# Kernel optimization log

Hardware: AMD Instinct MI355X
Metric: run time of the kernel (lower is better)

## Reference

```python
import jax, jax.numpy as jnp
import numpy as np

LN_EPS = 1e-9

def _layer_norm(x, g, b):
    mu = jnp.mean(x, axis=-1, keepdims=True)
    var = jnp.mean((x - mu) ** 2, axis=-1, keepdims=True)
    return (x - mu) * jax.lax.rsqrt(var + LN_EPS) * g + b

def _ffn(x, w1, b1, w2, b2, ln_g, ln_b):
    h = jax.nn.gelu(x @ w1 + b1, approximate=False)
    h = h @ w2 + b2
    return _layer_norm(h, ln_g, ln_b)

def _kernel_mean(x, y):
    d = x.shape[1]
    x2 = jnp.sum(x * x, axis=1)[:, None]
    y2 = jnp.sum(y * y, axis=1)[None, :]
    sq = x2 + y2 - 2.0 * (x @ y.T)  # [Nx, Ny]
    return jnp.mean(jnp.exp(-sq / (d * d)))

def _mmd(x, y):
    return _kernel_mean(x, x) + _kernel_mean(y, y) - 2.0 * _kernel_mean(x, y)

def setup_inputs() -> dict:
    key = jax.random.key(0)
    ks = jax.random.split(key, 8)
    B, S, D, DI, DL = 8, 512, 1024, 4096, 64
    s = lambda fan: 1.0 / np.sqrt(fan)
    return {
        "hidden": jax.random.normal(ks[0], (B, S, D), jnp.float32),
        "true_samples": jax.random.normal(ks[1], (B * S, DL), jnp.float32),
        "enc_w1": jax.random.normal(ks[2], (D, DI), jnp.float32) * s(D),
        "enc_b1": jnp.zeros((DI,), jnp.float32),
        "enc_w2": jax.random.normal(ks[3], (DI, DL), jnp.float32) * s(DI),
        "enc_b2": jnp.zeros((DL,), jnp.float32),
        "enc_ln_g": jnp.ones((DL,), jnp.float32),
        "enc_ln_b": jnp.zeros((DL,), jnp.float32),
        "dec_w1": jax.random.normal(ks[4], (DL, DI), jnp.float32) * s(DL),
        "dec_b1": jnp.zeros((DI,), jnp.float32),
        "dec_w2": jax.random.normal(ks[5], (DI, D), jnp.float32) * s(DI),
        "dec_b2": jnp.zeros((D,), jnp.float32),
        "dec_ln_g": jnp.ones((D,), jnp.float32),
        "dec_ln_b": jnp.zeros((D,), jnp.float32),
    }

def reference(hidden, true_samples, enc_w1, enc_b1, enc_w2, enc_b2, enc_ln_g, enc_ln_b,
              dec_w1, dec_b1, dec_w2, dec_b2, dec_ln_g, dec_ln_b):
    latent = _ffn(hidden, enc_w1, enc_b1, enc_w2, enc_b2, enc_ln_g, enc_ln_b)  # [B,S,DL]
    recon = _ffn(latent, dec_w1, dec_b1, dec_w2, dec_b2, dec_ln_g, dec_ln_b)   # [B,S,D]
    B, S, DL = latent.shape
    lat_flat = latent.reshape(-1, DL)  # [B*S, DL]
    reg_loss = _mmd(true_samples, lat_flat) / B * S
    return recon, latent, reg_loss
```

## Files before the change

### kernel.cpp

```cpp
#include <hip/hip_runtime.h>
#include <hip/hip_bf16.h>
#include <math.h>


typedef __attribute__((ext_vector_type(8))) short short8;
typedef __attribute__((ext_vector_type(4))) float float4a;
typedef __attribute__((ext_vector_type(4))) unsigned short us4;

__device__ inline ushort bf16r(float x) {
    union { float f; unsigned u; } c; c.f = x;
    unsigned r = (c.u + 0x7fffu + ((c.u >> 16) & 1u)) >> 16;
    return (ushort)r;
}

__device__ inline void gld_lds16(const void* g, void* l) {
    __builtin_amdgcn_global_load_lds(
        (const __attribute__((address_space(1))) void*)g,
        (__attribute__((address_space(3))) void*)l, 16, 0, 0);
}

template <int N> __device__ inline void wait_vmcnt() {
    if constexpr (N == 0) asm volatile("s_waitcnt vmcnt(0)" ::: "memory");
    else if constexpr (N == 4) asm volatile("s_waitcnt vmcnt(4)" ::: "memory");
    else if constexpr (N == 6) asm volatile("s_waitcnt vmcnt(6)" ::: "memory");
}

template <int N> __device__ inline void wait_lgkmcnt() {
    if constexpr (N == 0) asm volatile("s_waitcnt lgkmcnt(0)" ::: "memory");
    else if constexpr (N == 2) asm volatile("s_waitcnt lgkmcnt(2)" ::: "memory");
    else if constexpr (N == 4) asm volatile("s_waitcnt lgkmcnt(4)" ::: "memory");
    else if constexpr (N == 6) asm volatile("s_waitcnt lgkmcnt(6)" ::: "memory");
    else if constexpr (N == 8) asm volatile("s_waitcnt lgkmcnt(8)" ::: "memory");
    else if constexpr (N == 12) asm volatile("s_waitcnt lgkmcnt(12)" ::: "memory");
}

__device__ inline float fast_gelu(float v) {
    float v2 = v * v;
    float u = v * __builtin_fmaf(0.07135481627f, v2, 1.5957691216f);
    u = fminf(u, 30.0f);
    float e = __expf(u);
    return v * e * __builtin_amdgcn_rcpf(e + 1.0f);
}

__global__ __launch_bounds__(256) void k_pre(
        const float* __restrict__ hidden, ushort* __restrict__ A1bf,
        const float* __restrict__ tsamp, ushort* __restrict__ Tbf,
        float* __restrict__ sq_t, float* __restrict__ acc,
        const float* __restrict__ i0, ushort* __restrict__ o0,
        const float* __restrict__ i1, ushort* __restrict__ o1,
        const float* __restrict__ i2, ushort* __restrict__ o2,
        const float* __restrict__ i3, ushort* __restrict__ o3) {
    int b = blockIdx.x, tid = threadIdx.x;
    if (b == 0 && tid < 24) acc[tid] = 0.0f;
    if (b < 4096) {
        int i = b * 1024 + tid * 4;
        float4 v = *(const float4*)(hidden + i);
        us4 o = {bf16r(v.x), bf16r(v.y), bf16r(v.z), bf16r(v.w)};
        *(us4*)(A1bf + i) = o;
        return;
    }
    if (b < 4352) {
        int i = (b - 4096) * 1024 + tid * 4;
        float4 v = *(const float4*)(tsamp + i);
        us4 o = {bf16r(v.x), bf16r(v.y), bf16r(v.z), bf16r(v.w)};
        *(us4*)(Tbf + i) = o;
        float s = v.x * v.x + v.y * v.y + v.z * v.z + v.w * v.w;
#pragma unroll
        for (int off = 8; off; off >>= 1) s += __shfl_xor(s, off);
        if ((tid & 15) == 0) sq_t[i >> 6] = s;
        return;
    }
    __shared__ float t[32][65];
    const float* in; ushort* out; int R, C;
    int lb = b - 4352;
    if (lb < 2048)      { in = i0; out = o0; R = 1024; C = 4096; }
    else if (lb < 2176) { in = i1; out = o1; R = 4096; C = 64;   lb -= 2048; }
    else if (lb < 2304) { in = i2; out = o2; R = 64;   C = 4096; lb -= 2176; }
    else                { in = i3; out = o3; R = 4096; C = 1024; lb -= 2304; }
    int bx = (lb % (C / 32)) * 32;
    int by = (lb / (C / 32)) * 64;
    int tx = tid & 31, ty = tid >> 5;
#pragma unroll
    for (int i = 0; i < 64; i += 8)
        t[tx][i + ty] = in[(size_t)(by + i + ty) * C + (bx + tx)];
    __syncthreads();
#pragma unroll
    for (int i = 0; i < 32; i += 8) {
        int c = i + ty;
        ushort2 o;
        o.x = bf16r(t[c][2 * tx]);
        o.y = bf16r(t[c][2 * tx + 1]);
        *(ushort2*)(&out[(size_t)(bx + c) * R + by + 2 * tx]) = o;
    }
}

template <int BN, int EPI, bool SWZ>
__global__ __launch_bounds__(256) void k_gemm(
        const ushort* __restrict__ A, const ushort* __restrict__ Bt,
        const float* __restrict__ bias, void* __restrict__ Out,
        float* __restrict__ Out2, int M, int N, int K, int KC) {
    constexpr int BM = 128, BK = 64;
    constexpr int WAVES_N = BN / 64;
    constexpr int WAVES_M = 4 / WAVES_N;
    constexpr int WM = BM / WAVES_M;
    constexpr int MT = WM / 16;
    constexpr int NT = 4;
    constexpr int CA = BM / 32, CB = BN / 32;

    __shared__ ushort sA[BM * 64];
    __shared__ ushort sB[BN * 64];

    const int tid  = threadIdx.x;
    const int wave = tid >> 6, lane = tid & 63;
    const int wm = wave / WAVES_N, wn = wave % WAVES_N;
    int bx = blockIdx.x, by = blockIdx.y;
    if constexpr (SWZ) {
        int lin = blockIdx.x + gridDim.x * blockIdx.y;
        by = lin % gridDim.y;
        bx = lin / gridDim.y;
    }
    const int m0 = by * BM, n0 = bx * BN;
    const int lrow = lane & 15, lq = lane >> 4;
    const int srow8 = lane >> 3;
    const int sk8   = lane & 7;
    const int kbeg = blockIdx.z * KC;

    const ushort* pA[CA]; unsigned lA[CA];
#pragma unroll
    for (int j = 0; j < CA; ++j) {
        int c = wave * CA + j;
        int r = c * 8 + srow8;
        pA[j] = &A[(size_t)(m0 + r) * K + kbeg + ((sk8 ^ (r & 7)) * 8)];
        lA[j] = c * 512;
    }
    const ushort* pB[CB]; unsigned lB[CB];
#pragma unroll
    for (int j = 0; j < CB; ++j) {
        int c = wave * CB + j;
        int r = c * 8 + srow8;
        pB[j] = &Bt[(size_t)(n0 + r) * K + kbeg + ((sk8 ^ (r & 7)) * 8)];
        lB[j] = c * 512;
    }
    unsigned aoff[2][MT], boff[2][NT];
#pragma unroll
    for (int h = 0; h < 2; ++h) {
#pragma unroll
        for (int mt = 0; mt < MT; ++mt) {
            int r = wm * WM + mt * 16 + lrow;
            aoff[h][mt] = r * 64 + (((h * 4 + lq) ^ (r & 7)) * 8);
        }
#pragma unroll
        for (int nt = 0; nt < NT; ++nt) {
            int r = wn * 64 + nt * 16 + lrow;
            boff[h][nt] = r * 64 + (((h * 4 + lq) ^ (r & 7)) * 8);
        }
    }

    float4a acc[MT][NT];
#pragma unroll
    for (int mt = 0; mt < MT; ++mt)
#pragma unroll
        for (int nt = 0; nt < NT; ++nt)
            acc[mt][nt] = (float4a){0.f, 0.f, 0.f, 0.f};

    for (int k0 = 0; k0 < KC; k0 += BK) {
#pragma unroll
        for (int j = 0; j < CA; ++j) {
            gld_lds16(pA[j], &sA[lA[j]]);
            pA[j] += BK;
        }
#pragma unroll
        for (int j = 0; j < CB; ++j) {
            gld_lds16(pB[j], &sB[lB[j]]);
            pB[j] += BK;
        }
        __syncthreads();
#pragma unroll
        for (int h = 0; h < 2; ++h) {
            short8 af[MT], bfr[NT];
#pragma unroll
            for (int mt = 0; mt < MT; ++mt)
                af[mt] = *(short8*)(&sA[aoff[h][mt]]);
#pragma unroll
            for (int nt = 0; nt < NT; ++nt)
                bfr[nt] = *(short8*)(&sB[boff[h][nt]]);
#pragma unroll
            for (int mt = 0; mt < MT; ++mt)
#pragma unroll
                for (int nt = 0; nt < NT; ++nt)
                    acc[mt][nt] = __builtin_amdgcn_mfma_f32_16x16x32_bf16(
                        af[mt], bfr[nt], acc[mt][nt], 0, 0, 0);
        }
        __syncthreads();
    }

    float* dstp = nullptr;
    if constexpr (EPI == 2) {
        if (Out2 && blockIdx.z) dstp = Out2;
        else dstp = (float*)Out + (size_t)blockIdx.z * M * N;
    }
#pragma unroll
    for (int mt = 0; mt < MT; ++mt)
#pragma unroll
        for (int nt = 0; nt < NT; ++nt) {
            int col = n0 + wn * 64 + nt * 16 + lrow;
            float bv = 0.f;
            if constexpr (EPI != 2) bv = bias[col];
#pragma unroll
            for (int r = 0; r < 4; ++r) {
                int row = m0 + wm * WM + mt * 16 + lq * 4 + r;
                float v = acc[mt][nt][r] + bv;
                if constexpr (EPI == 0) {
                    ((ushort*)Out)[(size_t)row * N + col] = bf16r(fast_gelu(v));
                } else if constexpr (EPI == 1) {
                    ((float*)Out)[(size_t)row * N + col] = v;
                } else {
                    dstp[(size_t)row * N + col] = v;
                }
            }
        }
}

template <int BN, int EPI, int CX, int CY>
__global__ __launch_bounds__(512, 2) void k_gemm256mb(
        const ushort* __restrict__ A, const ushort* __restrict__ Bt,
        const float* __restrict__ bias, void* __restrict__ Out,
        float* __restrict__ Out2, int M, int N, int K, int KC) {
    constexpr int BM = 256, BK = 64;
    constexpr int AI = 4;
    constexpr int BI = BN / 64;
    constexpr int WAVES_N = BN / 64;
    constexpr int WAVES_M = 8 / WAVES_N;
    constexpr int WM = BM / WAVES_M;
    constexpr int MT = WM / 16;
    constexpr int NT = 4;

    __shared__ ushort sA[2][BM * 64];
    __shared__ ushort sB[2][BN * 64];

    const int tid = threadIdx.x;
    const int wave = tid >> 6, lane = tid & 63;
    const int wm = wave / WAVES_N, wn = wave % WAVES_N;

    const int gx = gridDim.x, gy = gridDim.y;
    const int lin = blockIdx.x + gx * (blockIdx.y + gy * blockIdx.z);
    const int nwg = gx * gy * gridDim.z;
    const int cpx = nwg >> 3;
    const int swz = (lin & 7) * cpx + (lin >> 3);
    const int nz  = gx * gy;
    const int zz  = swz / nz;
    const int rr  = swz % nz;
    const int chunk = rr / (CX * CY);
    const int lcl   = rr % (CX * CY);
    const int ncx   = gx / CX;
    const int bx = (chunk % ncx) * CX + (lcl % CX);
    const int by = (chunk / ncx) * CY + (lcl / CX);

    const int m0 = by * BM, n0 = bx * BN;
    const int lrow = lane & 15, lq = lane >> 4;
    const int kbeg = zz * KC;
    const int nT = KC / BK;

    const int crow = tid >> 3;
    const int ck8  = (tid & 7) ^ (crow & 7);
    const ushort* pAbase = A  + (size_t)(m0 + crow) * K + kbeg + ck8 * 8;
    const ushort* pBbase = Bt + (size_t)(n0 + crow) * K + kbeg + ck8 * 8;

    const int a0  = (wm * WM + lrow) * 64;
    const int b0  = (wn * 64 + lrow) * 64;
    const int sw0 = ((lq) ^ (lrow & 7)) * 8;
    const int sw1 = ((4 + lq) ^ (lrow & 7)) * 8;

    float4a acc[MT][NT];
#pragma unroll
    for (int mt = 0; mt < MT; ++mt)
#pragma unroll
        for (int nt = 0; nt < NT; ++nt)
            acc[mt][nt] = (float4a){0.f, 0.f, 0.f, 0.f};

#pragma unroll
    for (int j = 0; j < AI; ++j)
        gld_lds16(pAbase + (size_t)j * 64 * K, &sA[0][j * 4096 + wave * 512]);
#pragma unroll
    for (int j = 0; j < BI; ++j)
        gld_lds16(pBbase + (size_t)j * 64 * K, &sB[0][j * 4096 + wave * 512]);
    wait_vmcnt<0>();
    __builtin_amdgcn_s_barrier();
    __builtin_amdgcn_sched_barrier(0);

    for (int t = 0; t < nT; ++t) {
        const int d = t & 1;
        const bool pf1 = (t + 1 < nT);
        const size_t koff1 = (size_t)(t + 1) * BK;

        short8 af0[MT], bfr0[NT], af1[MT], bfr1[NT];
#pragma unroll
        for (int mt = 0; mt < MT; ++mt)
            af0[mt] = *(const short8*)(&sA[d][a0 + mt * 1024 + sw0]);
#pragma unroll
        for (int nt = 0; nt < NT; ++nt)
            bfr0[nt] = *(const short8*)(&sB[d][b0 + nt * 1024 + sw0]);
        __builtin_amdgcn_sched_barrier(0);
#pragma unroll
        for (int mt = 0; mt < MT; ++mt)
            af1[mt] = *(const short8*)(&sA[d][a0 + mt * 1024 + sw1]);
#pragma unroll
        for (int nt = 0; nt < NT; ++nt)
            bfr1[nt] = *(const short8*)(&sB[d][b0 + nt * 1024 + sw1]);
        if (pf1) {
#pragma unroll
            for (int j = 0; j < AI; ++j)
                gld_lds16(pAbase + (size_t)j * 64 * K + koff1,
                          &sA[d ^ 1][j * 4096 + wave * 512]);
#pragma unroll
            for (int j = 0; j < BI; ++j)
                gld_lds16(pBbase + (size_t)j * 64 * K + koff1,
                          &sB[d ^ 1][j * 4096 + wave * 512]);
        }
        wait_lgkmcnt<MT + 4>();
        __builtin_amdgcn_sched_barrier(0);
        __builtin_amdgcn_s_setprio(1);
#pragma unroll
        for (int mt = 0; mt < MT; ++mt)
#pragma unroll
            for (int nt = 0; nt < NT; ++nt)
                acc[mt][nt] = __builtin_amdgcn_mfma_f32_16x16x32_bf16(
                    af0[mt], bfr0[nt], acc[mt][nt], 0, 0, 0);
        __builtin_amdgcn_s_setprio(0);
        wait_lgkmcnt<0>();
        __builtin_amdgcn_sched_barrier(0);
        __builtin_amdgcn_s_setprio(1);
#pragma unroll
        for (int mt = 0; mt < MT; ++mt)
#pragma unroll
            for (int nt = 0; nt < NT; ++nt)
                acc[mt][nt] = __builtin_amdgcn_mfma_f32_16x16x32_bf16(
                    af1[mt], bfr1[nt], acc[mt][nt], 0, 0, 0);
        __builtin_amdgcn_s_setprio(0);
        if (pf1) {
            wait_vmcnt<0>();
            __builtin_amdgcn_s_barrier();
            __builtin_amdgcn_sched_barrier(0);
        }
    }

    float* dstp = nullptr;
    if constexpr (EPI == 2) {
        if (Out2 && zz) dstp = Out2;
        else dstp = (float*)Out + (size_t)zz * M * N;
    }
#pragma unroll
    for (int mt = 0; mt < MT; ++mt)
#pragma unroll
        for (int nt = 0; nt < NT; ++nt) {
            const int col = n0 + wn * 64 + nt * 16 + lrow;
            float bv = 0.f;
            if constexpr (EPI == 0) bv = bias[col];
#pragma unroll
            for (int r = 0; r < 4; ++r) {
                const int row = m0 + wm * WM + mt * 16 + lq * 4 + r;
                float v = acc[mt][nt][r] + bv;
                if constexpr (EPI == 0)
                    ((ushort*)Out)[(size_t)row * N + col] = bf16r(fast_gelu(v));
                else
                    dstp[(size_t)row * N + col] = v;
            }
        }
}

__global__ __launch_bounds__(512, 2) void k_gemm1f(
        const ushort* __restrict__ A, const ushort* __restrict__ Bt,
        const float* __restrict__ bias, const ushort* __restrict__ W2t,
        float* __restrict__ part, int M, int N, int K) {
    constexpr int BM = 256, BN = 256, BK = 64;
    constexpr int AI = 4, BI = 4;
    constexpr int WAVES_N = 4;
    constexpr int WM = 128;
    constexpr int MT = 8, NT = 4;
    constexpr int CX = 4, CY = 8;

    __shared__ ushort smem[65536];

    const int tid = threadIdx.x;
    const int wave = tid >> 6, lane = tid & 63;
    const int wm = wave / WAVES_N, wn = wave % WAVES_N;

    const int gx = gridDim.x, gy = gridDim.y;
    const int lin = blockIdx.x + gx * blockIdx.y;
    const int cpx = (gx * gy) >> 3;
    const int swz = (lin & 7) * cpx + (lin >> 3);
    const int chunk = swz / (CX * CY);
    const int lcl   = swz % (CX * CY);
    const int ncx   = gx / CX;
    const int bx = (chunk % ncx) * CX + (lcl % CX);
    const int by = (chunk / ncx) * CY + (lcl / CX);

    const int m0 = by * BM, n0 = bx * BN;
    const int lrow = lane & 15, lq = lane >> 4;
    const int nT = K / BK;

    const int crow = tid >> 3;
    const int ck8  = (tid & 7) ^ (crow & 7);
    const ushort* pAbase = A  + (size_t)(m0 + crow) * K + ck8 * 8;
    const ushort* pBbase = Bt + (size_t)(n0 + crow) * K + ck8 * 8;

    const int a0  = (wm * WM + lrow) * 64;
    const int b0  = (wn * 64 + lrow) * 64;
    const int sw0 = ((lq) ^ (lrow & 7)) * 8;
    const int sw1 = ((4 + lq) ^ (lrow & 7)) * 8;

    float4a acc[MT][NT];
#pragma unroll
    for (int mt = 0; mt < MT; ++mt)
#pragma unroll
        for (int nt = 0; nt < NT; ++nt)
            acc[mt][nt] = (float4a){0.f, 0.f, 0.f, 0.f};

#pragma unroll
    for (int j = 0; j < AI; ++j)
        gld_lds16(pAbase + (size_t)j * 64 * K, &smem[j * 4096 + wave * 512]);
#pragma unroll
    for (int j = 0; j < BI; ++j)
        gld_lds16(pBbase + (size_t)j * 64 * K,
                  &smem[32768 + j * 4096 + wave * 512]);
    wait_vmcnt<0>();
    __builtin_amdgcn_s_barrier();
    __builtin_amdgcn_sched_barrier(0);

    for (int t = 0; t < nT; ++t) {
        const int d = t & 1;
        const bool pf1 = (t + 1 < nT);
        const size_t koff1 = (size_t)(t + 1) * BK;
        const ushort* sAd = &smem[d * 16384];
        const ushort* sBd = &smem[32768 + d * 16384];

        short8 af0[MT], bfr0[NT], af1[MT], bfr1[NT];
#pragma unroll
        for (int mt = 0; mt < MT; ++mt)
            af0[mt] = *(const short8*)(&sAd[a0 + mt * 1024 + sw0]);
#pragma unroll
        for (int nt = 0; nt < NT; ++nt)
            bfr0[nt] = *(const short8*)(&sBd[b0 + nt * 1024 + sw0]);
        __builtin_amdgcn_sched_barrier(0);
#pragma unroll
        for (int mt = 0; mt < MT; ++mt)
            af1[mt] = *(const short8*)(&sAd[a0 + mt * 1024 + sw1]);
#pragma unroll
        for (int nt = 0; nt < NT; ++nt)
            bfr1[nt] = *(const short8*)(&sBd[b0 + nt * 1024 + sw1]);
        if (pf1) {
#pragma unroll
            for (int j = 0; j < AI; ++j)
                gld_lds16(pAbase + (size_t)j * 64 * K + koff1,
                          &smem[(d ^ 1) * 16384 + j * 4096 + wave * 512]);
#pragma unroll
            for (int j = 0; j < BI; ++j)
                gld_lds16(pBbase + (size_t)j * 64 * K + koff1,
                          &smem[32768 + (d ^ 1) * 16384 + j * 4096 + wave * 512]);
        }
        wait_lgkmcnt<12>();
        __builtin_amdgcn_sched_barrier(0);
        __builtin_amdgcn_s_setprio(1);
#pragma unroll
        for (int mt = 0; mt < MT; ++mt)
#pragma unroll
            for (int nt = 0; nt < NT; ++nt)
                acc[mt][nt] = __builtin_amdgcn_mfma_f32_16x16x32_bf16(
                    af0[mt], bfr0[nt], acc[mt][nt], 0, 0, 0);
        __builtin_amdgcn_s_setprio(0);
        wait_lgkmcnt<0>();
        __builtin_amdgcn_sched_barrier(0);
        __builtin_amdgcn_s_setprio(1);
#pragma unroll
        for (int mt = 0; mt < MT; ++mt)
#pragma unroll
            for (int nt = 0; nt < NT; ++nt)
                acc[mt][nt] = __builtin_amdgcn_mfma_f32_16x16x32_bf16(
                    af1[mt], bfr1[nt], acc[mt][nt], 0, 0, 0);
        __builtin_amdgcn_s_setprio(0);
        if (pf1) {
            wait_vmcnt<0>();
            __builtin_amdgcn_s_barrier();
            __builtin_amdgcn_sched_barrier(0);
        }
    }

    __syncthreads();
#pragma unroll
    for (int mt = 0; mt < MT; ++mt)
#pragma unroll
        for (int nt = 0; nt < NT; ++nt) {
            const int c = wn * 64 + nt * 16 + lrow;
            const float bv = bias[n0 + c];
            const int s = c >> 3, cl = c & 7;
#pragma unroll
            for (int r_ = 0; r_ < 4; ++r_) {
                const int r = wm * WM + mt * 16 + lq * 4 + r_;
                const int sz = (s & 24) | ((s & 7) ^ (r & 7));
                smem[r * 256 + sz * 8 + cl] =
                    bf16r(fast_gelu(acc[mt][nt][r_] + bv));
            }
        }
    __syncthreads();

    float4a pacc[2][4];
#pragma unroll
    for (int m2 = 0; m2 < 2; ++m2)
#pragma unroll
        for (int n2 = 0; n2 < 4; ++n2)
            pacc[m2][n2] = (float4a){0.f, 0.f, 0.f, 0.f};

    const ushort* gW2 = W2t + n0;
#pragma unroll
    for (int kk = 0; kk < 8; ++kk) {
        short8 af2[2], bf2[4];
#pragma unroll
        for (int m2 = 0; m2 < 2; ++m2) {
            const int r2 = wave * 32 + m2 * 16 + lrow;
            const int s2 = kk * 4 + lq;
            const int sz2 = (s2 & 24) | ((s2 & 7) ^ (r2 & 7));
            af2[m2] = *(const short8*)(&smem[r2 * 256 + sz2 * 8]);
        }
#pragma unroll
        for (int n2 = 0; n2 < 4; ++n2) {
            const int l = n2 * 16 + lrow;
            bf2[n2] = *(const short8*)(&gW2[(size_t)l * 4096 + kk * 32 + lq * 8]);
        }
#pragma unroll
        for (int m2 = 0; m2 < 2; ++m2)
#pragma unroll
            for (int n2 = 0; n2 < 4; ++n2)
                pacc[m2][n2] = __builtin_amdgcn_mfma_f32_16x16x32_bf16(
                    af2[m2], bf2[n2], pacc[m2][n2], 0, 0, 0);
    }

    float* pz = part + (size_t)bx * M * 64;
#pragma unroll
    for (int m2 = 0; m2 < 2; ++m2)
#pragma unroll
        for (int n2 = 0; n2 < 4; ++n2) {
            const int lat = n2 * 16 + lrow;
#pragma unroll
            for (int r_ = 0; r_ < 4; ++r_) {
                const int row = m0 + wave * 32 + m2 * 16 + lq * 4 + r_;
                pz[(size_t)row * 64 + lat] = pacc[m2][n2][r_];
            }
        }
}

__global__ __launch_bounds__(256) void k_gram_all(
        const ushort* __restrict__ Tbf, const ushort* __restrict__ Lbf,
        const float* __restrict__ sq_t, const float* __restrict__ sq_l,
        float* __restrict__ accum) {
    __shared__ ushort sX[128 * 64];
    __shared__ ushort sY[128 * 64];
    __shared__ float red[4];

    int id = blockIdx.x;
    int pair, tbx, tby; float w;
    if (id < 1056) {
        pair = (id < 528) ? 0 : 1;
        int t = (pair == 0) ? id : id - 528;
        int r = (int)((sqrtf(8.0f * t + 1.0f) - 1.0f) * 0.5f);
        while ((r + 1) * (r + 2) / 2 <= t) ++r;
        while (r * (r + 1) / 2 > t) --r;
        tby = r; tbx = t - r * (r + 1) / 2;
        w = (tbx == tby) ? 1.0f : 2.0f;
    } else {
        pair = 2; int t = id - 1056;
        tbx = t & 31; tby = t >> 5; w = 1.0f;
    }
    const ushort* Xb = (pair == 1) ? Lbf : Tbf;
    const ushort* Yb = (pair == 0) ? Tbf : Lbf;
    const float* sqX = (pair == 1) ? sq_l : sq_t;
    const float* sqY = (pair == 0) ? sq_t : sq_l;

    const int tid  = threadIdx.x;
    const int wave = tid >> 6, lane = tid & 63;
    const int wm = wave >> 1, wn = wave & 1;
    const int bx = tbx * 128, by = tby * 128;
    const int lrow = lane & 15, lq = lane >> 4;
    const int srow8 = lane >> 3, sk8 = lane & 7;

#pragma unroll
    for (int j = 0; j < 4; ++j) {
        int c = wave * 4 + j;
        int r = c * 8 + srow8;
        int kc = (sk8 ^ (r & 7)) * 8;
        gld_lds16(&Xb[(size_t)(bx + r) * 64 + kc], &sX[c * 512]);
        gld_lds16(&Yb[(size_t)(by + r) * 64 + kc], &sY[c * 512]);
    }

    unsigned xoff[2][4], yoff[2][4];
#pragma unroll
    for (int h = 0; h < 2; ++h)
#pragma unroll
        for (int i = 0; i < 4; ++i) {
            int rx = wm * 64 + i * 16 + lrow;
            int ry = wn * 64 + i * 16 + lrow;
            xoff[h][i] = rx * 64 + (((h * 4 + lq) ^ (rx & 7)) * 8);
            yoff[h][i] = ry * 64 + (((h * 4 + lq) ^ (ry & 7)) * 8);
        }
    __syncthreads();

    float4a acc[4][4];
#pragma unroll
    for (int mt = 0; mt < 4; ++mt)
#pragma unroll
        for (int nt = 0; nt < 4; ++nt)
            acc[mt][nt] = (float4a){0.f, 0.f, 0.f, 0.f};

#pragma unroll
    for (int h = 0; h < 2; ++h) {
        short8 xf[4], yf[4];
#pragma unroll
        for (int mt = 0; mt < 4; ++mt)
            xf[mt] = *(short8*)(&sX[xoff[h][mt]]);
#pragma unroll
        for (int nt = 0; nt < 4; ++nt)
            yf[nt] = *(short8*)(&sY[yoff[h][nt]]);
#pragma unroll
        for (int mt = 0; mt < 4; ++mt)
#pragma unroll
            for (int nt = 0; nt < 4; ++nt)
                acc[mt][nt] = __builtin_amdgcn_mfma_f32_16x16x32_bf16(
                    xf[mt], yf[nt], acc[mt][nt], 0, 0, 0);
    }

    float sy[4];
#pragma unroll
    for (int nt = 0; nt < 4; ++nt)
        sy[nt] = sqY[by + wn * 64 + nt * 16 + lrow];
    float s = 0.f;
#pragma unroll
    for (int mt = 0; mt < 4; ++mt)
#pragma unroll
        for (int r = 0; r < 4; ++r) {
            float sx = sqX[bx + wm * 64 + mt * 16 + lq * 4 + r];
#pragma unroll
            for (int nt = 0; nt < 4; ++nt)
                s += __expf((2.0f * acc[mt][nt][r] - sx - sy[nt]) * (1.0f / 4096.0f));
        }
    s *= w;
#pragma unroll
    for (int off = 32; off; off >>= 1) s += __shfl_xor(s, off);
    if ((tid & 63) == 0) red[tid >> 6] = s;
    __syncthreads();
    if (tid == 0) atomicAdd(accum + pair * 8, red[0] + red[1] + red[2] + red[3]);
}

__global__ __launch_bounds__(256) void k_ln64_red(
        const float* __restrict__ part, int npart,
        const float* __restrict__ bias, const float* __restrict__ g,
        const float* __restrict__ b, float* __restrict__ outf,
        ushort* __restrict__ outb, float* __restrict__ sq_l) {
    int wave = threadIdx.x >> 6, lane = threadIdx.x & 63;
    int row = blockIdx.x * 4 + wave;
    float x = bias[lane];
    for (int s = 0; s < npart; ++s)
        x += part[(size_t)s * 4096 * 64 + row * 64 + lane];
    float s = x;
#pragma unroll
    for (int off = 32; off; off >>= 1) s += __shfl_xor(s, off);
    float mu = s * (1.0f / 64.0f);
    float d = x - mu;
    float v = d * d;
#pragma unroll
    for (int off = 32; off; off >>= 1) v += __shfl_xor(v, off);
    float rs = rsqrtf(v * (1.0f / 64.0f) + 1e-9f);
    float y = d * rs * g[lane] + b[lane];
    outf[row * 64 + lane] = y;
    outb[row * 64 + lane] = bf16r(y);
    float q = y * y;
#pragma unroll
    for (int off = 32; off; off >>= 1) q += __shfl_xor(q, off);
    if (lane == 0) sq_l[row] = q;
}

__global__ __launch_bounds__(256) void k_ln1024_red(
        const float* __restrict__ p0, const float* __restrict__ p1,
        const float* __restrict__ bias, const float* __restrict__ g,
        const float* __restrict__ b, float* __restrict__ out) {
    __shared__ float red[4];
    int row = blockIdx.x, tid = threadIdx.x;
    const float4 v0 = *(const float4*)(p0 + (size_t)row * 1024 + tid * 4);
    const float4 v1 = *(const float4*)(p1 + (size_t)row * 1024 + tid * 4);
    const float4 bb = *(const float4*)(bias + tid * 4);
    float4 v;
    v.x = v0.x + v1.x + bb.x;
    v.y = v0.y + v1.y + bb.y;
    v.z = v0.z + v1.z + bb.z;
    v.w = v0.w + v1.w + bb.w;
    float s = v.x + v.y + v.z + v.w;
#pragma unroll
    for (int off = 32; off; off >>= 1) s += __shfl_xor(s, off);
    if ((tid & 63) == 0) red[tid >> 6] = s;
    __syncthreads();
    float mu = (red[0] + red[1] + red[2] + red[3]) * (1.0f / 1024.0f);
    float dx = v.x - mu, dy = v.y - mu, dz = v.z - mu, dw = v.w - mu;
    float q = dx * dx + dy * dy + dz * dz + dw * dw;
#pragma unroll
    for (int off = 32; off; off >>= 1) q += __shfl_xor(q, off);
    __syncthreads();
    if ((tid & 63) == 0) red[tid >> 6] = q;
    __syncthreads();
    float rs = rsqrtf((red[0] + red[1] + red[2] + red[3]) * (1.0f / 1024.0f) + 1e-9f);
    const float4 gv = *(const float4*)(g + tid * 4);
    const float4 bv = *(const float4*)(b + tid * 4);
    float4 o;
    o.x = dx * rs * gv.x + bv.x;
    o.y = dy * rs * gv.y + bv.y;
    o.z = dz * rs * gv.z + bv.z;
    o.w = dw * rs * gv.w + bv.w;
    *(float4*)(out + (size_t)row * 1024 + tid * 4) = o;
}

__global__ void k_finalize(const float* __restrict__ accum, float* __restrict__ out) {
    out[0] = (accum[0] + accum[8] - 2.0f * accum[16]) * (64.0f / (4096.0f * 4096.0f));
}

extern "C" void kernel_launch(void* const* d_in, const int* in_sizes, int n_in,
                              void* d_out, int out_size, void* d_ws, size_t ws_size,
                              hipStream_t stream) {
    const float* hidden   = (const float*)d_in[0];
    const float* tsamp    = (const float*)d_in[1];
    const float* enc_w1   = (const float*)d_in[2];
    const float* enc_b1   = (const float*)d_in[3];
    const float* enc_w2   = (const float*)d_in[4];
    const float* enc_b2   = (const float*)d_in[5];
    const float* enc_ln_g = (const float*)d_in[6];
    const float* enc_ln_b = (const float*)d_in[7];
    const float* dec_w1   = (const float*)d_in[8];
    const float* dec_b1   = (const float*)d_in[9];
    const float* dec_w2   = (const float*)d_in[10];
    const float* dec_b2   = (const float*)d_in[11];
    const float* dec_ln_g = (const float*)d_in[12];
    const float* dec_ln_b = (const float*)d_in[13];

    float* out      = (float*)d_out;
    float* recon    = out;
    float* latent_f = out + 4194304;
    float* reg      = out + 4456448;

    char* ws = (char*)d_ws;
    const size_t MB = 1024 * 1024;
    ushort* A1bf = (ushort*)(ws + 0);
    ushort* W1t  = (ushort*)(ws + 8 * MB);
    float*  h4p0 = (float*)(ws + 0);
    ushort* H1bf = (ushort*)(ws + 16 * MB);
    float*  part = (float*)(ws + 16 * MB);
    ushort* W4t  = (ushort*)(ws + 48 * MB);
    ushort* W2t  = (ushort*)(ws + 56 * MB);
    ushort* W3t  = (ushort*)(ws + 56 * MB + 512 * 1024);
    ushort* Lbf  = (ushort*)(ws + 57 * MB);
    float*  sq_t = (float*)(ws + 59 * MB);
    float*  sq_l = (float*)(ws + 59 * MB + 16384);
    float*  acc3 = (float*)(ws + 59 * MB + 32768);
    ushort* Tbf  = (ushort*)(ws + 59 * MB + 65536);

    k_pre<<<8704, 256, 0, stream>>>(hidden, A1bf, tsamp, Tbf, sq_t, acc3,
                                    enc_w1, W1t, enc_w2, W2t,
                                    dec_w1, W3t, dec_w2, W4t);

    k_gemm1f<<<dim3(16, 16, 1), 512, 0, stream>>>(
        A1bf, W1t, enc_b1, W2t, part, 4096, 4096, 1024);
    k_ln64_red<<<1024, 256, 0, stream>>>(part, 16, enc_b2, enc_ln_g, enc_ln_b,
                                         latent_f, Lbf, sq_l);

    k_gemm<64, 0, false><<<dim3(64, 32, 1), 256, 0, stream>>>(
        Lbf, W3t, dec_b1, H1bf, nullptr, 4096, 4096, 64, 64);
    k_gemm256mb<128, 2, 8, 4><<<dim3(8, 16, 2), 512, 0, stream>>>(
        H1bf, W4t, nullptr, h4p0, recon, 4096, 1024, 4096, 2048);
    k_ln1024_red<<<4096, 256, 0, stream>>>(h4p0, recon, dec_b2, dec_ln_g,
                                           dec_ln_b, recon);

    k_gram_all<<<2080, 256, 0, stream>>>(Tbf, Lbf, sq_t, sq_l, acc3);
    k_finalize<<<1, 1, 0, stream>>>(acc3, reg);
}
```

Before: 260.6 us.

## Fuse whole pipeline into one cooperative persistent kernel with grid syncs

```diff
diff --git a/kernel.cpp b/kernel.cpp
--- a/kernel.cpp
+++ b/kernel.cpp
@@ -1,7 +1,10 @@
 #include <hip/hip_runtime.h>
+#include <hip/hip_cooperative_groups.h>
 #include <hip/hip_bf16.h>
 #include <math.h>
 
+
+namespace cg = cooperative_groups;
 
 typedef __attribute__((ext_vector_type(8))) short short8;
 typedef __attribute__((ext_vector_type(4))) float float4a;
@@ -21,16 +24,10 @@
 
 template <int N> __device__ inline void wait_vmcnt() {
     if constexpr (N == 0) asm volatile("s_waitcnt vmcnt(0)" ::: "memory");
-    else if constexpr (N == 4) asm volatile("s_waitcnt vmcnt(4)" ::: "memory");
-    else if constexpr (N == 6) asm volatile("s_waitcnt vmcnt(6)" ::: "memory");
 }
 
 template <int N> __device__ inline void wait_lgkmcnt() {
     if constexpr (N == 0) asm volatile("s_waitcnt lgkmcnt(0)" ::: "memory");
-    else if constexpr (N == 2) asm volatile("s_waitcnt lgkmcnt(2)" ::: "memory");
-    else if constexpr (N == 4) asm volatile("s_waitcnt lgkmcnt(4)" ::: "memory");
-    else if constexpr (N == 6) asm volatile("s_waitcnt lgkmcnt(6)" ::: "memory");
-    else if constexpr (N == 8) asm volatile("s_waitcnt lgkmcnt(8)" ::: "memory");
     else if constexpr (N == 12) asm volatile("s_waitcnt lgkmcnt(12)" ::: "memory");
 }
 
@@ -42,681 +39,631 @@
     return v * e * __builtin_amdgcn_rcpf(e + 1.0f);
 }
 
-__global__ __launch_bounds__(256) void k_pre(
-        const float* __restrict__ hidden, ushort* __restrict__ A1bf,
-        const float* __restrict__ tsamp, ushort* __restrict__ Tbf,
-        float* __restrict__ sq_t, float* __restrict__ acc,
-        const float* __restrict__ i0, ushort* __restrict__ o0,
-        const float* __restrict__ i1, ushort* __restrict__ o1,
-        const float* __restrict__ i2, ushort* __restrict__ o2,
-        const float* __restrict__ i3, ushort* __restrict__ o3) {
-    int b = blockIdx.x, tid = threadIdx.x;
-    if (b == 0 && tid < 24) acc[tid] = 0.0f;
-    if (b < 4096) {
-        int i = b * 1024 + tid * 4;
-        float4 v = *(const float4*)(hidden + i);
-        us4 o = {bf16r(v.x), bf16r(v.y), bf16r(v.z), bf16r(v.w)};
-        *(us4*)(A1bf + i) = o;
-        return;
+__global__ __launch_bounds__(512, 2) void k_mega(
+        const float* __restrict__ hidden, const float* __restrict__ tsamp,
+        const float* __restrict__ ew1, const float* __restrict__ eb1,
+        const float* __restrict__ ew2, const float* __restrict__ eb2,
+        const float* __restrict__ elng, const float* __restrict__ elnb,
+        const float* __restrict__ dw1, const float* __restrict__ db1,
+        const float* __restrict__ dw2, const float* __restrict__ db2,
+        const float* __restrict__ dlng, const float* __restrict__ dlnb,
+        float* __restrict__ recon, float* __restrict__ latent_f,
+        float* __restrict__ regout,
+        ushort* __restrict__ A1bf, ushort* __restrict__ W1t,
+        float* __restrict__ part, float* __restrict__ h4p0,
+        ushort* __restrict__ H1bf, ushort* __restrict__ W4t,
+        ushort* __restrict__ W2t, ushort* __restrict__ W3t,
+        ushort* __restrict__ Lbf, float* __restrict__ sq_t,
+        float* __restrict__ sq_l, float* __restrict__ acc3,
+        ushort* __restrict__ Tbf) {
+    __shared__ char smem_u[131072];
+    cg::grid_group grid = cg::this_grid();
+
+    const int bid = blockIdx.x;
+    const int tid = threadIdx.x;
+    const int wave = tid >> 6, lane = tid & 63;
+    const int htid = tid & 255, half = tid >> 8;
+    const int lrow = lane & 15, lq = lane >> 4;
+    const int srow8 = lane >> 3, sk8 = lane & 7;
+
+    {
+        if (bid == 0 && tid < 32) acc3[tid] = 0.0f;
+#pragma unroll
+        for (int it = 0; it < 8; ++it) {
+            int i4 = it * 131072 + bid * 512 + tid;
+            float4 v = ((const float4*)hidden)[i4];
+            us4 o = {bf16r(v.x), bf16r(v.y), bf16r(v.z), bf16r(v.w)};
+            ((us4*)A1bf)[i4] = o;
+        }
+        {
+            int gw = bid * 8 + wave;
+            if (gw < 1024) {
+                int row = gw * 4 + (lane >> 4);
+                int i = row * 64 + (lane & 15) * 4;
+                float4 v = *(const float4*)(tsamp + i);
+                us4 o = {bf16r(v.x), bf16r(v.y), bf16r(v.z), bf16r(v.w)};
+                *(us4*)(Tbf + i) = o;
+                float s = v.x * v.x + v.y * v.y + v.z * v.z + v.w * v.w;
+#pragma unroll
+                for (int off = 8; off; off >>= 1) s += __shfl_xor(s, off);
+                if ((lane & 15) == 0) sq_t[row] = s;
+            }
+        }
+        float (*tT)[65] = (float(*)[65])(smem_u + half * 8320);
+        int tx = htid & 31, ty = htid >> 5;
+        for (int it = 0; it < 9; ++it) {
+            int vt = (bid + it * 256) * 2 + half;
+            bool act = vt < 4352;
+            const float* in = nullptr; ushort* out = nullptr; int R = 1, C = 32;
+            int lb = vt;
+            if (act) {
+                if (lb < 2048)      { in = ew1; out = W1t; R = 1024; C = 4096; }
+                else if (lb < 2176) { in = ew2; out = W2t; R = 4096; C = 64;   lb -= 2048; }
+                else if (lb < 2304) { in = dw1; out = W3t; R = 64;   C = 4096; lb -= 2176; }
+                else                { in = dw2; out = W4t; R = 4096; C = 1024; lb -= 2304; }
+            }
+            int bx = act ? (lb % (C / 32)) * 32 : 0;
+            int by = act ? (lb / (C / 32)) * 64 : 0;
+            if (act) {
+#pragma unroll
+                for (int i = 0; i < 64; i += 8)
+                    tT[tx][i + ty] = in[(size_t)(by + i + ty) * C + (bx + tx)];
+            }
+            __syncthreads();
+            if (act) {
+#pragma unroll
+                for (int i = 0; i < 32; i += 8) {
+                    int c = i + ty;
+                    ushort2 o;
+                    o.x = bf16r(tT[c][2 * tx]);
+                    o.y = bf16r(tT[c][2 * tx + 1]);
+                    *(ushort2*)(&out[(size_t)(bx + c) * R + by + 2 * tx]) = o;
+                }
+            }
+            __syncthreads();
+        }
     }
-    if (b < 4352) {
-        int i = (b - 4096) * 1024 + tid * 4;
-        float4 v = *(const float4*)(tsamp + i);
-        us4 o = {bf16r(v.x), bf16r(v.y), bf16r(v.z), bf16r(v.w)};
-        *(us4*)(Tbf + i) = o;
-        float s = v.x * v.x + v.y * v.y + v.z * v.z + v.w * v.w;
-#pragma unroll
-        for (int off = 8; off; off >>= 1) s += __shfl_xor(s, off);
-        if ((tid & 15) == 0) sq_t[i >> 6] = s;
-        return;
-    }
-    __shared__ float t[32][65];
-    const float* in; ushort* out; int R, C;
-    int lb = b - 4352;
-    if (lb < 2048)      { in = i0; out = o0; R = 1024; C = 4096; }
-    else if (lb < 2176) { in = i1; out = o1; R = 4096; C = 64;   lb -= 2048; }
-    else if (lb < 2304) { in = i2; out = o2; R = 64;   C = 4096; lb -= 2176; }
-    else                { in = i3; out = o3; R = 4096; C = 1024; lb -= 2304; }
-    int bx = (lb % (C / 32)) * 32;
-    int by = (lb / (C / 32)) * 64;
-    int tx = tid & 31, ty = tid >> 5;
-#pragma unroll
-    for (int i = 0; i < 64; i += 8)
-        t[tx][i + ty] = in[(size_t)(by + i + ty) * C + (bx + tx)];
-    __syncthreads();
-#pragma unroll
-    for (int i = 0; i < 32; i += 8) {
-        int c = i + ty;
-        ushort2 o;
-        o.x = bf16r(t[c][2 * tx]);
-        o.y = bf16r(t[c][2 * tx + 1]);
-        *(ushort2*)(&out[(size_t)(bx + c) * R + by + 2 * tx]) = o;
-    }
-}
-
-template <int BN, int EPI, bool SWZ>
-__global__ __launch_bounds__(256) void k_gemm(
-        const ushort* __restrict__ A, const ushort* __restrict__ Bt,
-        const float* __restrict__ bias, void* __restrict__ Out,
-        float* __restrict__ Out2, int M, int N, int K, int KC) {
-    constexpr int BM = 128, BK = 64;
-    constexpr int WAVES_N = BN / 64;
-    constexpr int WAVES_M = 4 / WAVES_N;
-    constexpr int WM = BM / WAVES_M;
-    constexpr int MT = WM / 16;
-    constexpr int NT = 4;
-    constexpr int CA = BM / 32, CB = BN / 32;
-
-    __shared__ ushort sA[BM * 64];
-    __shared__ ushort sB[BN * 64];
-
-    const int tid  = threadIdx.x;
-    const int wave = tid >> 6, lane = tid & 63;
-    const int wm = wave / WAVES_N, wn = wave % WAVES_N;
-    int bx = blockIdx.x, by = blockIdx.y;
-    if constexpr (SWZ) {
-        int lin = blockIdx.x + gridDim.x * blockIdx.y;
-        by = lin % gridDim.y;
-        bx = lin / gridDim.y;
-    }
-    const int m0 = by * BM, n0 = bx * BN;
-    const int lrow = lane & 15, lq = lane >> 4;
-    const int srow8 = lane >> 3;
-    const int sk8   = lane & 7;
-    const int kbeg = blockIdx.z * KC;
-
-    const ushort* pA[CA]; unsigned lA[CA];
-#pragma unroll
-    for (int j = 0; j < CA; ++j) {
-        int c = wave * CA + j;
-        int r = c * 8 + srow8;
-        pA[j] = &A[(size_t)(m0 + r) * K + kbeg + ((sk8 ^ (r & 7)) * 8)];
-        lA[j] = c * 512;
-    }
-    const ushort* pB[CB]; unsigned lB[CB];
-#pragma unroll
-    for (int j = 0; j < CB; ++j) {
-        int c = wave * CB + j;
-        int r = c * 8 + srow8;
-        pB[j] = &Bt[(size_t)(n0 + r) * K + kbeg + ((sk8 ^ (r & 7)) * 8)];
-        lB[j] = c * 512;
-    }
-    unsigned aoff[2][MT], boff[2][NT];
-#pragma unroll
-    for (int h = 0; h < 2; ++h) {
-#pragma unroll
-        for (int mt = 0; mt < MT; ++mt) {
-            int r = wm * WM + mt * 16 + lrow;
-            aoff[h][mt] = r * 64 + (((h * 4 + lq) ^ (r & 7)) * 8);
-        }
-#pragma unroll
-        for (int nt = 0; nt < NT; ++nt) {
-            int r = wn * 64 + nt * 16 + lrow;
-            boff[h][nt] = r * 64 + (((h * 4 + lq) ^ (r & 7)) * 8);
-        }
-    }
-
-    float4a acc[MT][NT];
-#pragma unroll
-    for (int mt = 0; mt < MT; ++mt)
-#pragma unroll
-        for (int nt = 0; nt < NT; ++nt)
-            acc[mt][nt] = (float4a){0.f, 0.f, 0.f, 0.f};
-
-    for (int k0 = 0; k0 < KC; k0 += BK) {
-#pragma unroll
-        for (int j = 0; j < CA; ++j) {
-            gld_lds16(pA[j], &sA[lA[j]]);
-            pA[j] += BK;
-        }
-#pragma unroll
-        for (int j = 0; j < CB; ++j) {
-            gld_lds16(pB[j], &sB[lB[j]]);
-            pB[j] += BK;
-        }
-        __syncthreads();
-#pragma unroll
-        for (int h = 0; h < 2; ++h) {
-            short8 af[MT], bfr[NT];
+    __threadfence();
+    grid.sync();
+
+    {
+        constexpr int AI = 4, BI = 4, MT = 8, NT = 4;
+        constexpr int WM = 128, CX = 4, CY = 8;
+        ushort* smem = (ushort*)smem_u;
+        const int wm = wave / 4, wn = wave % 4;
+        const int lin = bid;
+        const int cpx = 256 >> 3;
+        const int swz = (lin & 7) * cpx + (lin >> 3);
+        const int chunk = swz / (CX * CY);
+        const int lcl   = swz % (CX * CY);
+        const int ncx   = 16 / CX;
+        const int bx = (chunk % ncx) * CX + (lcl % CX);
+        const int by = (chunk / ncx) * CY + (lcl / CX);
+        const int m0 = by * 256, n0 = bx * 256;
+        const int K = 1024, nT = 16;
+
+        const int crow = tid >> 3;
+        const int ck8  = (tid & 7) ^ (crow & 7);
+        const ushort* pAbase = A1bf + (size_t)(m0 + crow) * K + ck8 * 8;
+        const ushort* pBbase = W1t  + (size_t)(n0 + crow) * K + ck8 * 8;
+
+        const int a0  = (wm * WM + lrow) * 64;
+        const int b0  = (wn * 64 + lrow) * 64;
+        const int sw0 = ((lq) ^ (lrow & 7)) * 8;
+        const int sw1 = ((4 + lq) ^ (lrow & 7)) * 8;
+
+        float4a acc[MT][NT];
+#pragma unroll
+        for (int mt = 0; mt < MT; ++mt)
+#pragma unroll
+            for (int nt = 0; nt < NT; ++nt)
+                acc[mt][nt] = (float4a){0.f, 0.f, 0.f, 0.f};
+
+#pragma unroll
+        for (int j = 0; j < AI; ++j)
+            gld_lds16(pAbase + (size_t)j * 64 * K, &smem[j * 4096 + wave * 512]);
+#pragma unroll
+        for (int j = 0; j < BI; ++j)
+            gld_lds16(pBbase + (size_t)j * 64 * K,
+                      &smem[32768 + j * 4096 + wave * 512]);
+        wait_vmcnt<0>();
+        __builtin_amdgcn_s_barrier();
+        __builtin_amdgcn_sched_barrier(0);
+
+        for (int t = 0; t < nT; ++t) {
+            const int d = t & 1;
+            const bool pf1 = (t + 1 < nT);
+            const size_t koff1 = (size_t)(t + 1) * 64;
+            const ushort* sAd = &smem[d * 16384];
+            const ushort* sBd = &smem[32768 + d * 16384];
+
+            short8 af0[MT], bfr0[NT], af1[MT], bfr1[NT];
 #pragma unroll
             for (int mt = 0; mt < MT; ++mt)
-                af[mt] = *(short8*)(&sA[aoff[h][mt]]);
+                af0[mt] = *(const short8*)(&sAd[a0 + mt * 1024 + sw0]);
 #pragma unroll
             for (int nt = 0; nt < NT; ++nt)
-                bfr[nt] = *(short8*)(&sB[boff[h][nt]]);
+                bfr0[nt] = *(const short8*)(&sBd[b0 + nt * 1024 + sw0]);
+            __builtin_amdgcn_sched_barrier(0);
+#pragma unroll
+            for (int mt = 0; mt < MT; ++mt)
+                af1[mt] = *(const short8*)(&sAd[a0 + mt * 1024 + sw1]);
+#pragma unroll
+            for (int nt = 0; nt < NT; ++nt)
+                bfr1[nt] = *(const short8*)(&sBd[b0 + nt * 1024 + sw1]);
+            if (pf1) {
+#pragma unroll
+                for (int j = 0; j < AI; ++j)
+                    gld_lds16(pAbase + (size_t)j * 64 * K + koff1,
+                              &smem[(d ^ 1) * 16384 + j * 4096 + wave * 512]);
+#pragma unroll
+                for (int j = 0; j < BI; ++j)
+                    gld_lds16(pBbase + (size_t)j * 64 * K + koff1,
+                              &smem[32768 + (d ^ 1) * 16384 + j * 4096 + wave * 512]);
+            }
+            wait_lgkmcnt<12>();
+            __builtin_amdgcn_sched_barrier(0);
+            __builtin_amdgcn_s_setprio(1);
 #pragma unroll
             for (int mt = 0; mt < MT; ++mt)
 #pragma unroll
                 for (int nt = 0; nt < NT; ++nt)
                     acc[mt][nt] = __builtin_amdgcn_mfma_f32_16x16x32_bf16(
-                        af[mt], bfr[nt], acc[mt][nt], 0, 0, 0);
-        }
+                        af0[mt], bfr0[nt], acc[mt][nt], 0, 0, 0);
+            __builtin_amdgcn_s_setprio(0);
+            wait_lgkmcnt<0>();
+            __builtin_amdgcn_sched_barrier(0);
+            __builtin_amdgcn_s_setprio(1);
+#pragma unroll
+            for (int mt = 0; mt < MT; ++mt)
+#pragma unroll
+                for (int nt = 0; nt < NT; ++nt)
+                    acc[mt][nt] = __builtin_amdgcn_mfma_f32_16x16x32_bf16(
+                        af1[mt], bfr1[nt], acc[mt][nt], 0, 0, 0);
+            __builtin_amdgcn_s_setprio(0);
+            if (pf1) {
+                wait_vmcnt<0>();
+                __builtin_amdgcn_s_barrier();
+                __builtin_amdgcn_sched_barrier(0);
+            }
+        }
+
         __syncthreads();
+#pragma unroll
+        for (int mt = 0; mt < MT; ++mt)
+#pragma unroll
+            for (int nt = 0; nt < NT; ++nt) {
+                const int c = wn * 64 + nt * 16 + lrow;
+                const float bv = eb1[n0 + c];
+                const int s = c >> 3, cl = c & 7;
+#pragma unroll
+                for (int r_ = 0; r_ < 4; ++r_) {
+                    const int r = wm * WM + mt * 16 + lq * 4 + r_;
+                    const int sz = (s & 24) | ((s & 7) ^ (r & 7));
+                    smem[r * 256 + sz * 8 + cl] =
+                        bf16r(fast_gelu(acc[mt][nt][r_] + bv));
+                }
+            }
+        __syncthreads();
+
+        float4a pacc[2][4];
+#pragma unroll
+        for (int m2 = 0; m2 < 2; ++m2)
+#pragma unroll
+            for (int n2 = 0; n2 < 4; ++n2)
+                pacc[m2][n2] = (float4a){0.f, 0.f, 0.f, 0.f};
+
+        const ushort* gW2 = W2t + n0;
+#pragma unroll
+        for (int kk = 0; kk < 8; ++kk) {
+            short8 af2[2], bf2[4];
+#pragma unroll
+            for (int m2 = 0; m2 < 2; ++m2) {
+                const int r2 = wave * 32 + m2 * 16 + lrow;
+                const int s2 = kk * 4 + lq;
+                const int sz2 = (s2 & 24) | ((s2 & 7) ^ (r2 & 7));
+                af2[m2] = *(const short8*)(&smem[r2 * 256 + sz2 * 8]);
+            }
+#pragma unroll
+            for (int n2 = 0; n2 < 4; ++n2) {
+                const int l = n2 * 16 + lrow;
+                bf2[n2] = *(const short8*)(&gW2[(size_t)l * 4096 + kk * 32 + lq * 8]);
+            }
+#pragma unroll
+            for (int m2 = 0; m2 < 2; ++m2)
+#pragma unroll
+                for (int n2 = 0; n2 < 4; ++n2)
+                    pacc[m2][n2] = __builtin_amdgcn_mfma_f32_16x16x32_bf16(
+                        af2[m2], bf2[n2], pacc[m2][n2], 0, 0, 0);
+        }
+
+        float* pz = part + (size_t)bx * 4096 * 64;
+#pragma unroll
+        for (int m2 = 0; m2 < 2; ++m2)
+#pragma unroll
+            for (int n2 = 0; n2 < 4; ++n2) {
+                const int lat = n2 * 16 + lrow;
+#pragma unroll
+                for (int r_ = 0; r_ < 4; ++r_) {
+                    const int row = m0 + wave * 32 + m2 * 16 + lq * 4 + r_;
+                    pz[(size_t)row * 64 + lat] = pacc[m2][n2][r_];
+                }
+            }
     }
-
-    float* dstp = nullptr;
-    if constexpr (EPI == 2) {
-        if (Out2 && blockIdx.z) dstp = Out2;
-        else dstp = (float*)Out + (size_t)blockIdx.z * M * N;
+    __threadfence();
+    grid.sync();
+
+    {
+        int gw = bid * 8 + wave;
+#pragma unroll
+        for (int rr = 0; rr < 2; ++rr) {
+            int row = gw + rr * 2048;
+            float x = eb2[lane];
+            for (int s = 0; s < 16; ++s)
+                x += part[(size_t)s * 4096 * 64 + row * 64 + lane];
+            float s = x;
+#pragma unroll
+            for (int off = 32; off; off >>= 1) s += __shfl_xor(s, off);
+            float mu = s * (1.0f / 64.0f);
+            float dxx = x - mu;
+            float v = dxx * dxx;
+#pragma unroll
+            for (int off = 32; off; off >>= 1) v += __shfl_xor(v, off);
+            float rs = rsqrtf(v * (1.0f / 64.0f) + 1e-9f);
+            float y = dxx * rs * elng[lane] + elnb[lane];
+            latent_f[row * 64 + lane] = y;
+            Lbf[row * 64 + lane] = bf16r(y);
+            float q = y * y;
+#pragma unroll
+            for (int off = 32; off; off >>= 1) q += __shfl_xor(q, off);
+            if (lane == 0) sq_l[row] = q;
+        }
     }
-#pragma unroll
-    for (int mt = 0; mt < MT; ++mt)
-#pragma unroll
-        for (int nt = 0; nt < NT; ++nt) {
-            int col = n0 + wn * 64 + nt * 16 + lrow;
-            float bv = 0.f;
-            if constexpr (EPI != 2) bv = bias[col];
-#pragma unroll
-            for (int r = 0; r < 4; ++r) {
-                int row = m0 + wm * WM + mt * 16 + lq * 4 + r;
-                float v = acc[mt][nt][r] + bv;
-                if constexpr (EPI == 0) {
-                    ((ushort*)Out)[(size_t)row * N + col] = bf16r(fast_gelu(v));
-                } else if constexpr (EPI == 1) {
-                    ((float*)Out)[(size_t)row * N + col] = v;
+    __threadfence();
+    grid.sync();
+
+    {
+        ushort* sA3 = (ushort*)(smem_u + half * 24576);
+        ushort* sB3 = sA3 + 8192;
+        const int w4 = htid >> 6, hl = htid & 63;
+        const int hlrow = hl & 15, hlq = hl >> 4;
+        const int hsr8 = hl >> 3, hsk8 = hl & 7;
+        for (int it = 0; it < 4; ++it) {
+            int vt = (bid * 2 + half) + it * 512;
+            int bx3 = vt & 63, by3 = vt >> 6;
+            int m0 = by3 * 128, n0 = bx3 * 64;
+#pragma unroll
+            for (int j = 0; j < 4; ++j) {
+                int c = w4 * 4 + j;
+                int r = c * 8 + hsr8;
+                gld_lds16(&Lbf[(size_t)(m0 + r) * 64 + ((hsk8 ^ (r & 7)) * 8)],
+                          &sA3[c * 512]);
+            }
+#pragma unroll
+            for (int j = 0; j < 2; ++j) {
+                int c = w4 * 2 + j;
+                int r = c * 8 + hsr8;
+                gld_lds16(&W3t[(size_t)(n0 + r) * 64 + ((hsk8 ^ (r & 7)) * 8)],
+                          &sB3[c * 512]);
+            }
+            __syncthreads();
+            float4a a3[2][4];
+#pragma unroll
+            for (int mt = 0; mt < 2; ++mt)
+#pragma unroll
+                for (int nt = 0; nt < 4; ++nt)
+                    a3[mt][nt] = (float4a){0.f, 0.f, 0.f, 0.f};
+#pragma unroll
+            for (int h = 0; h < 2; ++h) {
+                short8 af[2], bfr[4];
+#pragma unroll
+                for (int mt = 0; mt < 2; ++mt) {
+                    int r = w4 * 32 + mt * 16 + hlrow;
+                    af[mt] = *(short8*)(&sA3[r * 64 + (((h * 4 + hlq) ^ (r & 7)) * 8)]);
+                }
+#pragma unroll
+                for (int nt = 0; nt < 4; ++nt) {
+                    int r = nt * 16 + hlrow;
+                    bfr[nt] = *(short8*)(&sB3[r * 64 + (((h * 4 + hlq) ^ (r & 7)) * 8)]);
+                }
+#pragma unroll
+                for (int mt = 0; mt < 2; ++mt)
+#pragma unroll
+                    for (int nt = 0; nt < 4; ++nt)
+                        a3[mt][nt] = __builtin_amdgcn_mfma_f32_16x16x32_bf16(
+                            af[mt], bfr[nt], a3[mt][nt], 0, 0, 0);
+            }
+            __syncthreads();
+#pragma unroll
+            for (int mt = 0; mt < 2; ++mt)
+#pragma unroll
+                for (int nt = 0; nt < 4; ++nt) {
+                    int col = n0 + nt * 16 + hlrow;
+                    float bv = db1[col];
+#pragma unroll
+                    for (int r_ = 0; r_ < 4; ++r_) {
+                        int row = m0 + w4 * 32 + mt * 16 + hlq * 4 + r_;
+                        H1bf[(size_t)row * 4096 + col] =
+                            bf16r(fast_gelu(a3[mt][nt][r_] + bv));
+                    }
+                }
+        }
+    }
+    __threadfence();
+    grid.sync();
+
+    {
+        constexpr int AI = 4, BI = 2, MT = 4, NT = 4, WM = 64;
+        constexpr int CX = 8, CY = 4;
+        ushort* sA4 = (ushort*)smem_u;
+        ushort* sB4 = (ushort*)(smem_u + 65536);
+        const int wm = wave / 2, wn = wave % 2;
+        const int gx = 8, gy = 16;
+        const int lin = bid;
+        const int cpx = 256 >> 3;
+        const int swz = (lin & 7) * cpx + (lin >> 3);
+        const int nz  = gx * gy;
+        const int zz  = swz / nz;
+        const int rr  = swz % nz;
+        const int chunk = rr / (CX * CY);
+        const int lcl   = rr % (CX * CY);
+        const int ncx   = gx / CX;
+        const int bx = (chunk % ncx) * CX + (lcl % CX);
+        const int by = (chunk / ncx) * CY + (lcl / CX);
+        const int m0 = by * 256, n0 = bx * 128;
+        const int K = 4096, KC = 2048, nT = 32;
+        const int kbeg = zz * KC;
+
+        const int crow = tid >> 3;
+        const int ck8  = (tid & 7) ^ (crow & 7);
+        const ushort* pAbase = H1bf + (size_t)(m0 + crow) * K + kbeg + ck8 * 8;
+        const ushort* pBbase = W4t  + (size_t)(n0 + crow) * K + kbeg + ck8 * 8;
+
+        const int a0  = (wm * WM + lrow) * 64;
+        const int b0  = (wn * 64 + lrow) * 64;
+        const int sw0 = ((lq) ^ (lrow & 7)) * 8;
+        const int sw1 = ((4 + lq) ^ (lrow & 7)) * 8;
+
+        float4a acc[MT][NT];
+#pragma unroll
+        for (int mt = 0; mt < MT; ++mt)
+#pragma unroll
+            for (int nt = 0; nt < NT; ++nt)
+                acc[mt][nt] = (float4a){0.f, 0.f, 0.f, 0.f};
+
+#pragma unroll
+        for (int j = 0; j < AI; ++j)
+            gld_lds16(pAbase + (size_t)j * 64 * K, &sA4[j * 4096 + wave * 512]);
+#pragma unroll
+        for (int j = 0; j < BI; ++j)
+            gld_lds16(pBbase + (size_t)j * 64 * K, &sB4[j * 4096 + wave * 512]);
+        wait_vmcnt<0>();
+        __builtin_amdgcn_s_barrier();
+        __builtin_amdgcn_sched_barrier(0);
+
+        for (int t = 0; t < nT; ++t) {
+            const int d = t & 1;
+            const bool pf1 = (t + 1 < nT);
+            const size_t koff1 = (size_t)(t + 1) * 64;
+            const ushort* sAd = &sA4[d * 16384];
+            const ushort* sBd = &sB4[d * 8192];
+
+            short8 af0[MT], bfr0[NT], af1[MT], bfr1[NT];
+#pragma unroll
+            for (int mt = 0; mt < MT; ++mt)
+                af0[mt] = *(const short8*)(&sAd[a0 + mt * 1024 + sw0]);
+#pragma unroll
+            for (int nt = 0; nt < NT; ++nt)
+                bfr0[nt] = *(const short8*)(&sBd[b0 + nt * 1024 + sw0]);
+            __builtin_amdgcn_sched_barrier(0);
+#pragma unroll
+            for (int mt = 0; mt < MT; ++mt)
+                af1[mt] = *(const short8*)(&sAd[a0 + mt * 1024 + sw1]);
+#pragma unroll
+            for (int nt = 0; nt < NT; ++nt)
+                bfr1[nt] = *(const short8*)(&sBd[b0 + nt * 1024 + sw1]);
+            if (pf1) {
+#pragma unroll
+                for (int j = 0; j < AI; ++j)
+                    gld_lds16(pAbase + (size_t)j * 64 * K + koff1,
+                              &sA4[(d ^ 1) * 16384 + j * 4096 + wave * 512]);
+#pragma unroll
+                for (int j = 0; j < BI; ++j)
+                    gld_lds16(pBbase + (size_t)j * 64 * K + koff1,
+                              &sB4[(d ^ 1) * 8192 + j * 4096 + wave * 512]);
+            }
+            wait_lgkmcnt<12>();
+            __builtin_amdgcn_sched_barrier(0);
+            __builtin_amdgcn_s_setprio(1);
+#pragma unroll
+            for (int mt = 0; mt < MT; ++mt)
+#pragma unroll
+                for (int nt = 0; nt < NT; ++nt)
+                    acc[mt][nt] = __builtin_amdgcn_mfma_f32_16x16x32_bf16(
+                        af0[mt], bfr0[nt], acc[mt][nt], 0, 0, 0);
+            __builtin_amdgcn_s_setprio(0);
+            wait_lgkmcnt<0>();
+            __builtin_amdgcn_sched_barrier(0);
+            __builtin_amdgcn_s_setprio(1);
+#pragma unroll
+            for (int mt = 0; mt < MT; ++mt)
+#pragma unroll
+                for (int nt = 0; nt < NT; ++nt)
+                    acc[mt][nt] = __builtin_amdgcn_mfma_f32_16x16x32_bf16(
+                        af1[mt], bfr1[nt], acc[mt][nt], 0, 0, 0);
+            __builtin_amdgcn_s_setprio(0);
+            if (pf1) {
+                wait_vmcnt<0>();
+                __builtin_amdgcn_s_barrier();
+                __builtin_amdgcn_sched_barrier(0);
+            }
+        }
+
+        float* dstp = zz ? recon : h4p0;
+#pragma unroll
+        for (int mt = 0; mt < MT; ++mt)
+#pragma unroll
+            for (int nt = 0; nt < NT; ++nt) {
+                const int col = n0 + wn * 64 + nt * 16 + lrow;
+#pragma unroll
+                for (int r_ = 0; r_ < 4; ++r_) {
+                    const int row = m0 + wm * WM + mt * 16 + lq * 4 + r_;
+                    dstp[(size_t)row * 1024 + col] = acc[mt][nt][r_];
+                }
+            }
+    }
+    __threadfence();
+    grid.sync();
+
+    {
+        float* red5 = (float*)smem_u + half * 4;
+        for (int it = 0; it < 8; ++it) {
+            int row = (bid * 2 + half) + it * 512;
+            const float4 v0 = *(const float4*)(h4p0 + (size_t)row * 1024 + htid * 4);
+            const float4 v1 = *(const float4*)(recon + (size_t)row * 1024 + htid * 4);
+            const float4 bb = *(const float4*)(db2 + htid * 4);
+            float4 v;
+            v.x = v0.x + v1.x + bb.x;
+            v.y = v0.y + v1.y + bb.y;
+            v.z = v0.z + v1.z + bb.z;
+            v.w = v0.w + v1.w + bb.w;
+            float s = v.x + v.y + v.z + v.w;
+#pragma unroll
+            for (int off = 32; off; off >>= 1) s += __shfl_xor(s, off);
+            if ((htid & 63) == 0) red5[htid >> 6] = s;
+            __syncthreads();
+            float mu = (red5[0] + red5[1] + red5[2] + red5[3]) * (1.0f / 1024.0f);
+            float dx = v.x - mu, dy = v.y - mu, dz = v.z - mu, dw = v.w - mu;
+            float q = dx * dx + dy * dy + dz * dz + dw * dw;
+#pragma unroll
+            for (int off = 32; off; off >>= 1) q += __shfl_xor(q, off);
+            __syncthreads();
+            if ((htid & 63) == 0) red5[htid >> 6] = q;
+            __syncthreads();
+            float rs = rsqrtf((red5[0] + red5[1] + red5[2] + red5[3]) *
+                              (1.0f / 1024.0f) + 1e-9f);
+            const float4 gv = *(const float4*)(dlng + htid * 4);
+            const float4 bv = *(const float4*)(dlnb + htid * 4);
+            float4 o;
+            o.x = dx * rs * gv.x + bv.x;
+            o.y = dy * rs * gv.y + bv.y;
+            o.z = dz * rs * gv.z + bv.z;
+            o.w = dw * rs * gv.w + bv.w;
+            *(float4*)(recon + (size_t)row * 1024 + htid * 4) = o;
+            __syncthreads();
+        }
+    }
+    __threadfence();
+    grid.sync();
+
+    {
+        ushort* sX = (ushort*)(smem_u + half * 32768);
+        ushort* sY = sX + 8192;
+        float* red6 = (float*)(smem_u + 65536) + half * 4;
+        const int w4 = htid >> 6, hl = htid & 63;
+        const int hlrow = hl & 15, hlq = hl >> 4;
+        const int hsr8 = hl >> 3, hsk8 = hl & 7;
+        const int wmg = w4 >> 1, wng = w4 & 1;
+
+        for (int it = 0; it < 5; ++it) {
+            int id = (bid * 2 + half) + it * 512;
+            bool act = id < 2080;
+            int pair = 0, tbx = 0, tby = 0; float w = 1.0f;
+            const ushort *Xb = Tbf, *Yb = Tbf;
+            const float *sqX = sq_t, *sqY = sq_t;
+            if (act) {
+                if (id < 1056) {
+                    pair = (id < 528) ? 0 : 1;
+                    int t = (pair == 0) ? id : id - 528;
+                    int r = (int)((sqrtf(8.0f * t + 1.0f) - 1.0f) * 0.5f);
+                    while ((r + 1) * (r + 2) / 2 <= t) ++r;
+                    while (r * (r + 1) / 2 > t) --r;
+                    tby = r; tbx = t - r * (r + 1) / 2;
+                    w = (tbx == tby) ? 1.0f : 2.0f;
                 } else {
-                    dstp[(size_t)row * N + col] = v;
-                }
-            }
-        }
-}
-
-template <int BN, int EPI, int CX, int CY>
-__global__ __launch_bounds__(512, 2) void k_gemm256mb(
-        const ushort* __restrict__ A, const ushort* __restrict__ Bt,
-        const float* __restrict__ bias, void* __restrict__ Out,
-        float* __restrict__ Out2, int M, int N, int K, int KC) {
-    constexpr int BM = 256, BK = 64;
-    constexpr int AI = 4;
-    constexpr int BI = BN / 64;
-    constexpr int WAVES_N = BN / 64;
-    constexpr int WAVES_M = 8 / WAVES_N;
-    constexpr int WM = BM / WAVES_M;
-    constexpr int MT = WM / 16;
-    constexpr int NT = 4;
-
-    __shared__ ushort sA[2][BM * 64];
-    __shared__ ushort sB[2][BN * 64];
-
-    const int tid = threadIdx.x;
-    const int wave = tid >> 6, lane = tid & 63;
-    const int wm = wave / WAVES_N, wn = wave % WAVES_N;
-
-    const int gx = gridDim.x, gy = gridDim.y;
-    const int lin = blockIdx.x + gx * (blockIdx.y + gy * blockIdx.z);
-    const int nwg = gx * gy * gridDim.z;
-    const int cpx = nwg >> 3;
-    const int swz = (lin & 7) * cpx + (lin >> 3);
-    const int nz  = gx * gy;
-    const int zz  = swz / nz;
-    const int rr  = swz % nz;
-    const int chunk = rr / (CX * CY);
-    const int lcl   = rr % (CX * CY);
-    const int ncx   = gx / CX;
-    const int bx = (chunk % ncx) * CX + (lcl % CX);
-    const int by = (chunk / ncx) * CY + (lcl / CX);
-
-    const int m0 = by * BM, n0 = bx * BN;
-    const int lrow = lane & 15, lq = lane >> 4;
-    const int kbeg = zz * KC;
-    const int nT = KC / BK;
-
-    const int crow = tid >> 3;
-    const int ck8  = (tid & 7) ^ (crow & 7);
-    const ushort* pAbase = A  + (size_t)(m0 + crow) * K + kbeg + ck8 * 8;
-    const ushort* pBbase = Bt + (size_t)(n0 + crow) * K + kbeg + ck8 * 8;
-
-    const int a0  = (wm * WM + lrow) * 64;
-    const int b0  = (wn * 64 + lrow) * 64;
-    const int sw0 = ((lq) ^ (lrow & 7)) * 8;
-    const int sw1 = ((4 + lq) ^ (lrow & 7)) * 8;
-
-    float4a acc[MT][NT];
-#pragma unroll
-    for (int mt = 0; mt < MT; ++mt)
-#pragma unroll
-        for (int nt = 0; nt < NT; ++nt)
-            acc[mt][nt] = (float4a){0.f, 0.f, 0.f, 0.f};
-
-#pragma unroll
-    for (int j = 0; j < AI; ++j)
-        gld_lds16(pAbase + (size_t)j * 64 * K, &sA[0][j * 4096 + wave * 512]);
-#pragma unroll
-    for (int j = 0; j < BI; ++j)
-        gld_lds16(pBbase + (size_t)j * 64 * K, &sB[0][j * 4096 + wave * 512]);
-    wait_vmcnt<0>();
-    __builtin_amdgcn_s_barrier();
-    __builtin_amdgcn_sched_barrier(0);
-
-    for (int t = 0; t < nT; ++t) {
-        const int d = t & 1;
-        const bool pf1 = (t + 1 < nT);
-        const size_t koff1 = (size_t)(t + 1) * BK;
-
-        short8 af0[MT], bfr0[NT], af1[MT], bfr1[NT];
-#pragma unroll
-        for (int mt = 0; mt < MT; ++mt)
-            af0[mt] = *(const short8*)(&sA[d][a0 + mt * 1024 + sw0]);
-#pragma unroll
-        for (int nt = 0; nt < NT; ++nt)
-            bfr0[nt] = *(const short8*)(&sB[d][b0 + nt * 1024 + sw0]);
-        __builtin_amdgcn_sched_barrier(0);
-#pragma unroll
-        for (int mt = 0; mt < MT; ++mt)
-            af1[mt] = *(const short8*)(&sA[d][a0 + mt * 1024 + sw1]);
-#pragma unroll
-        for (int nt = 0; nt < NT; ++nt)
-            bfr1[nt] = *(const short8*)(&sB[d][b0 + nt * 1024 + sw1]);
-        if (pf1) {
-#pragma unroll
-            for (int j = 0; j < AI; ++j)
-                gld_lds16(pAbase + (size_t)j * 64 * K + koff1,
-                          &sA[d ^ 1][j * 4096 + wave * 512]);
-#pragma unroll
-            for (int j = 0; j < BI; ++j)
-                gld_lds16(pBbase + (size_t)j * 64 * K + koff1,
-                          &sB[d ^ 1][j * 4096 + wave * 512]);
-        }
-        wait_lgkmcnt<MT + 4>();
-        __builtin_amdgcn_sched_barrier(0);
-        __builtin_amdgcn_s_setprio(1);
-#pragma unroll
-        for (int mt = 0; mt < MT; ++mt)
-#pragma unroll
-            for (int nt = 0; nt < NT; ++nt)
-                acc[mt][nt] = __builtin_amdgcn_mfma_f32_16x16x32_bf16(
-                    af0[mt], bfr0[nt], acc[mt][nt], 0, 0, 0);
-        __builtin_amdgcn_s_setprio(0);
-        wait_lgkmcnt<0>();
-        __builtin_amdgcn_sched_barrier(0);
-        __builtin_amdgcn_s_setprio(1);
-#pragma unroll
-        for (int mt = 0; mt < MT; ++mt)
-#pragma unroll
-            for (int nt = 0; nt < NT; ++nt)
-                acc[mt][nt] = __builtin_amdgcn_mfma_f32_16x16x32_bf16(
-                    af1[mt], bfr1[nt], acc[mt][nt], 0, 0, 0);
-        __builtin_amdgcn_s_setprio(0);
-        if (pf1) {
-            wait_vmcnt<0>();
-            __builtin_amdgcn_s_barrier();
-            __builtin_amdgcn_sched_barrier(0);
+                    pair = 2; int t = id - 1056;
+                    tbx = t & 31; tby = t >> 5; w = 1.0f;
+                }
+                Xb = (pair == 1) ? Lbf : Tbf;
+                Yb = (pair == 0) ? Tbf : Lbf;
+                sqX = (pair == 1) ? sq_l : sq_t;
+                sqY = (pair == 0) ? sq_t : sq_l;
+            }
+            const int bx = tbx * 128, by = tby * 128;
+            if (act) {
+#pragma unroll
+                for (int j = 0; j < 4; ++j) {
+                    int c = w4 * 4 + j;
+                    int r = c * 8 + hsr8;
+                    int kc = (hsk8 ^ (r & 7)) * 8;
+                    gld_lds16(&Xb[(size_t)(bx + r) * 64 + kc], &sX[c * 512]);
+                    gld_lds16(&Yb[(size_t)(by + r) * 64 + kc], &sY[c * 512]);
+                }
+            }
+            __syncthreads();
+            float s = 0.f;
+            if (act) {
+                float4a ag[4][4];
+#pragma unroll
+                for (int mt = 0; mt < 4; ++mt)
+#pragma unroll
+                    for (int nt = 0; nt < 4; ++nt)
+                        ag[mt][nt] = (float4a){0.f, 0.f, 0.f, 0.f};
+#pragma unroll
+                for (int h = 0; h < 2; ++h) {
+                    short8 xf[4], yf[4];
+#pragma unroll
+                    for (int mt = 0; mt < 4; ++mt) {
+                        int rx = wmg * 64 + mt * 16 + hlrow;
+                        xf[mt] = *(short8*)(&sX[rx * 64 + (((h * 4 + hlq) ^ (rx & 7)) * 8)]);
+                    }
+#pragma unroll
+                    for (int nt = 0; nt < 4; ++nt) {
+                        int ry = wng * 64 + nt * 16 + hlrow;
+                        yf[nt] = *(short8*)(&sY[ry * 64 + (((h * 4 + hlq) ^ (ry & 7)) * 8)]);
+                    }
+#pragma unroll
+                    for (int mt = 0; mt < 4; ++mt)
+#pragma unroll
+                        for (int nt = 0; nt < 4; ++nt)
+                            ag[mt][nt] = __builtin_amdgcn_mfma_f32_16x16x32_bf16(
+                                xf[mt], yf[nt], ag[mt][nt], 0, 0, 0);
+                }
+                float sy[4];
+#pragma unroll
+                for (int nt = 0; nt < 4; ++nt)
+                    sy[nt] = sqY[by + wng * 64 + nt * 16 + hlrow];
+#pragma unroll
+                for (int mt = 0; mt < 4; ++mt)
+#pragma unroll
+                    for (int r = 0; r < 4; ++r) {
+                        float sx = sqX[bx + wmg * 64 + mt * 16 + hlq * 4 + r];
+#pragma unroll
+                        for (int nt = 0; nt < 4; ++nt)
+                            s += __expf((2.0f * ag[mt][nt][r] - sx - sy[nt]) *
+                                        (1.0f / 4096.0f));
+                    }
+                s *= w;
+#pragma unroll
+                for (int off = 32; off; off >>= 1) s += __shfl_xor(s, off);
+                if (hl == 0) red6[w4] = s;
+            }
+            __syncthreads();
+            if (act && htid == 0) {
+                atomicAdd(acc3 + pair * 8, red6[0] + red6[1] + red6[2] + red6[3]);
+                __threadfence();
+                unsigned prev = atomicAdd((unsigned*)(acc3 + 24), 1u);
+                if (prev == 2079) {
+                    float a0 = atomicAdd(acc3 + 0, 0.0f);
+                    float a1 = atomicAdd(acc3 + 8, 0.0f);
+                    float a2 = atomicAdd(acc3 + 16, 0.0f);
+                    regout[0] = (a0 + a1 - 2.0f * a2) *
+                                (64.0f / (4096.0f * 4096.0f));
+                }
+            }
+            __syncthreads();
         }
     }
-
-    float* dstp = nullptr;
-    if constexpr (EPI == 2) {
-        if (Out2 && zz) dstp = Out2;
-        else dstp = (float*)Out + (size_t)zz * M * N;
-    }
-#pragma unroll
-    for (int mt = 0; mt < MT; ++mt)
-#pragma unroll
-        for (int nt = 0; nt < NT; ++nt) {
-            const int col = n0 + wn * 64 + nt * 16 + lrow;
-            float bv = 0.f;
-            if constexpr (EPI == 0) bv = bias[col];
-#pragma unroll
-            for (int r = 0; r < 4; ++r) {
-                const int row = m0 + wm * WM + mt * 16 + lq * 4 + r;
-                float v = acc[mt][nt][r] + bv;
-                if constexpr (EPI == 0)
-                    ((ushort*)Out)[(size_t)row * N + col] = bf16r(fast_gelu(v));
-                else
-                    dstp[(size_t)row * N + col] = v;
-            }
-        }
-}
-
-__global__ __launch_bounds__(512, 2) void k_gemm1f(
-        const ushort* __restrict__ A, const ushort* __restrict__ Bt,
-        const float* __restrict__ bias, const ushort* __restrict__ W2t,
-        float* __restrict__ part, int M, int N, int K) {
-    constexpr int BM = 256, BN = 256, BK = 64;
-    constexpr int AI = 4, BI = 4;
-    constexpr int WAVES_N = 4;
-    constexpr int WM = 128;
-    constexpr int MT = 8, NT = 4;
-    constexpr int CX = 4, CY = 8;
-
-    __shared__ ushort smem[65536];
-
-    const int tid = threadIdx.x;
-    const int wave = tid >> 6, lane = tid & 63;
-    const int wm = wave / WAVES_N, wn = wave % WAVES_N;
-
-    const int gx = gridDim.x, gy = gridDim.y;
-    const int lin = blockIdx.x + gx * blockIdx.y;
-    const int cpx = (gx * gy) >> 3;
-    const int swz = (lin & 7) * cpx + (lin >> 3);
-    const int chunk = swz / (CX * CY);
-    const int lcl   = swz % (CX * CY);
-    const int ncx   = gx / CX;
-    const int bx = (chunk % ncx) * CX + (lcl % CX);
-    const int by = (chunk / ncx) * CY + (lcl / CX);
-
-    const int m0 = by * BM, n0 = bx * BN;
-    const int lrow = lane & 15, lq = lane >> 4;
-    const int nT = K / BK;
-
-    const int crow = tid >> 3;
-    const int ck8  = (tid & 7) ^ (crow & 7);
-    const ushort* pAbase = A  + (size_t)(m0 + crow) * K + ck8 * 8;
-    const ushort* pBbase = Bt + (size_t)(n0 + crow) * K + ck8 * 8;
-
-    const int a0  = (wm * WM + lrow) * 64;
-    const int b0  = (wn * 64 + lrow) * 64;
-    const int sw0 = ((lq) ^ (lrow & 7)) * 8;
-    const int sw1 = ((4 + lq) ^ (lrow & 7)) * 8;
-
-    float4a acc[MT][NT];
-#pragma unroll
-    for (int mt = 0; mt < MT; ++mt)
-#pragma unroll
-        for (int nt = 0; nt < NT; ++nt)
-            acc[mt][nt] = (float4a){0.f, 0.f, 0.f, 0.f};
-
-#pragma unroll
-    for (int j = 0; j < AI; ++j)
-        gld_lds16(pAbase + (size_t)j * 64 * K, &smem[j * 4096 + wave * 512]);
-#pragma unroll
-    for (int j = 0; j < BI; ++j)
-        gld_lds16(pBbase + (size_t)j * 64 * K,
-                  &smem[32768 + j * 4096 + wave * 512]);
-    wait_vmcnt<0>();
-    __builtin_amdgcn_s_barrier();
-    __builtin_amdgcn_sched_barrier(0);
-
-    for (int t = 0; t < nT; ++t) {
-        const int d = t & 1;
-        const bool pf1 = (t + 1 < nT);
-        const size_t koff1 = (size_t)(t + 1) * BK;
-        const ushort* sAd = &smem[d * 16384];
-        const ushort* sBd = &smem[32768 + d * 16384];
-
-        short8 af0[MT], bfr0[NT], af1[MT], bfr1[NT];
-#pragma unroll
-        for (int mt = 0; mt < MT; ++mt)
-            af0[mt] = *(const short8*)(&sAd[a0 + mt * 1024 + sw0]);
-#pragma unroll
-        for (int nt = 0; nt < NT; ++nt)
-            bfr0[nt] = *(const short8*)(&sBd[b0 + nt * 1024 + sw0]);
-        __builtin_amdgcn_sched_barrier(0);
-#pragma unroll
-        for (int mt = 0; mt < MT; ++mt)
-            af1[mt] = *(const short8*)(&sAd[a0 + mt * 1024 + sw1]);
-#pragma unroll
-        for (int nt = 0; nt < NT; ++nt)
-            bfr1[nt] = *(const short8*)(&sBd[b0 + nt * 1024 + sw1]);
-        if (pf1) {
-#pragma unroll
-            for (int j = 0; j < AI; ++j)
-                gld_lds16(pAbase + (size_t)j * 64 * K + koff1,
-                          &smem[(d ^ 1) * 16384 + j * 4096 + wave * 512]);
-#pragma unroll
-            for (int j = 0; j < BI; ++j)
-                gld_lds16(pBbase + (size_t)j * 64 * K + koff1,
-                          &smem[32768 + (d ^ 1) * 16384 + j * 4096 + wave * 512]);
-        }
-        wait_lgkmcnt<12>();
-        __builtin_amdgcn_sched_barrier(0);
-        __builtin_amdgcn_s_setprio(1);
-#pragma unroll
-        for (int mt = 0; mt < MT; ++mt)
-#pragma unroll
-            for (int nt = 0; nt < NT; ++nt)
-                acc[mt][nt] = __builtin_amdgcn_mfma_f32_16x16x32_bf16(
-                    af0[mt], bfr0[nt], acc[mt][nt], 0, 0, 0);
-        __builtin_amdgcn_s_setprio(0);
-        wait_lgkmcnt<0>();
-        __builtin_amdgcn_sched_barrier(0);
-        __builtin_amdgcn_s_setprio(1);
-#pragma unroll
-        for (int mt = 0; mt < MT; ++mt)
-#pragma unroll
-            for (int nt = 0; nt < NT; ++nt)
-                acc[mt][nt] = __builtin_amdgcn_mfma_f32_16x16x32_bf16(
-                    af1[mt], bfr1[nt], acc[mt][nt], 0, 0, 0);
-        __builtin_amdgcn_s_setprio(0);
-        if (pf1) {
-            wait_vmcnt<0>();
-            __builtin_amdgcn_s_barrier();
-            __builtin_amdgcn_sched_barrier(0);
-        }
-    }
-
-    __syncthreads();
-#pragma unroll
-    for (int mt = 0; mt < MT; ++mt)
-#pragma unroll
-        for (int nt = 0; nt < NT; ++nt) {
-            const int c = wn * 64 + nt * 16 + lrow;
-            const float bv = bias[n0 + c];
-            const int s = c >> 3, cl = c & 7;
-#pragma unroll
-            for (int r_ = 0; r_ < 4; ++r_) {
-                const int r = wm * WM + mt * 16 + lq * 4 + r_;
-                const int sz = (s & 24) | ((s & 7) ^ (r & 7));
-                smem[r * 256 + sz * 8 + cl] =
-                    bf16r(fast_gelu(acc[mt][nt][r_] + bv));
-            }
-        }
-    __syncthreads();
-
-    float4a pacc[2][4];
-#pragma unroll
-    for (int m2 = 0; m2 < 2; ++m2)
-#pragma unroll
-        for (int n2 = 0; n2 < 4; ++n2)
-            pacc[m2][n2] = (float4a){0.f, 0.f, 0.f, 0.f};
-
-    const ushort* gW2 = W2t + n0;
-#pragma unroll
-    for (int kk = 0; kk < 8; ++kk) {
-        short8 af2[2], bf2[4];
-#pragma unroll
-        for (int m2 = 0; m2 < 2; ++m2) {
-            const int r2 = wave * 32 + m2 * 16 + lrow;
-            const int s2 = kk * 4 + lq;
-            const int sz2 = (s2 & 24) | ((s2 & 7) ^ (r2 & 7));
-            af2[m2] = *(const short8*)(&smem[r2 * 256 + sz2 * 8]);
-        }
-#pragma unroll
-        for (int n2 = 0; n2 < 4; ++n2) {
-            const int l = n2 * 16 + lrow;
-            bf2[n2] = *(const short8*)(&gW2[(size_t)l * 4096 + kk * 32 + lq * 8]);
-        }
-#pragma unroll
-        for (int m2 = 0; m2 < 2; ++m2)
-#pragma unroll
-            for (int n2 = 0; n2 < 4; ++n2)
-                pacc[m2][n2] = __builtin_amdgcn_mfma_f32_16x16x32_bf16(
-                    af2[m2], bf2[n2], pacc[m2][n2], 0, 0, 0);
-    }
-
-    float* pz = part + (size_t)bx * M * 64;
-#pragma unroll
-    for (int m2 = 0; m2 < 2; ++m2)
-#pragma unroll
-        for (int n2 = 0; n2 < 4; ++n2) {
-            const int lat = n2 * 16 + lrow;
-#pragma unroll
-            for (int r_ = 0; r_ < 4; ++r_) {
-                const int row = m0 + wave * 32 + m2 * 16 + lq * 4 + r_;
-                pz[(size_t)row * 64 + lat] = pacc[m2][n2][r_];
-            }
-        }
-}
-
-__global__ __launch_bounds__(256) void k_gram_all(
-        const ushort* __restrict__ Tbf, const ushort* __restrict__ Lbf,
-        const float* __restrict__ sq_t, const float* __restrict__ sq_l,
-        float* __restrict__ accum) {
-    __shared__ ushort sX[128 * 64];
-    __shared__ ushort sY[128 * 64];
-    __shared__ float red[4];
-
-    int id = blockIdx.x;
-    int pair, tbx, tby; float w;
-    if (id < 1056) {
-        pair = (id < 528) ? 0 : 1;
-        int t = (pair == 0) ? id : id - 528;
-        int r = (int)((sqrtf(8.0f * t + 1.0f) - 1.0f) * 0.5f);
-        while ((r + 1) * (r + 2) / 2 <= t) ++r;
-        while (r * (r + 1) / 2 > t) --r;
-        tby = r; tbx = t - r * (r + 1) / 2;
-        w = (tbx == tby) ? 1.0f : 2.0f;
-    } else {
-        pair = 2; int t = id - 1056;
-        tbx = t & 31; tby = t >> 5; w = 1.0f;
-    }
-    const ushort* Xb = (pair == 1) ? Lbf : Tbf;
-    const ushort* Yb = (pair == 0) ? Tbf : Lbf;
-    const float* sqX = (pair == 1) ? sq_l : sq_t;
-    const float* sqY = (pair == 0) ? sq_t : sq_l;
-
-    const int tid  = threadIdx.x;
-    const int wave = tid >> 6, lane = tid & 63;
-    const int wm = wave >> 1, wn = wave & 1;
-    const int bx = tbx * 128, by = tby * 128;
-    const int lrow = lane & 15, lq = lane >> 4;
-    const int srow8 = lane >> 3, sk8 = lane & 7;
-
-#pragma unroll
-    for (int j = 0; j < 4; ++j) {
-        int c = wave * 4 + j;
-        int r = c * 8 + srow8;
-        int kc = (sk8 ^ (r & 7)) * 8;
-        gld_lds16(&Xb[(size_t)(bx + r) * 64 + kc], &sX[c * 512]);
-        gld_lds16(&Yb[(size_t)(by + r) * 64 + kc], &sY[c * 512]);
-    }
-
-    unsigned xoff[2][4], yoff[2][4];
-#pragma unroll
-    for (int h = 0; h < 2; ++h)
-#pragma unroll
-        for (int i = 0; i < 4; ++i) {
-            int rx = wm * 64 + i * 16 + lrow;
-            int ry = wn * 64 + i * 16 + lrow;
-            xoff[h][i] = rx * 64 + (((h * 4 + lq) ^ (rx & 7)) * 8);
-            yoff[h][i] = ry * 64 + (((h * 4 + lq) ^ (ry & 7)) * 8);
-        }
-    __syncthreads();
-
-    float4a acc[4][4];
-#pragma unroll
-    for (int mt = 0; mt < 4; ++mt)
-#pragma unroll
-        for (int nt = 0; nt < 4; ++nt)
-            acc[mt][nt] = (float4a){0.f, 0.f, 0.f, 0.f};
-
-#pragma unroll
-    for (int h = 0; h < 2; ++h) {
-        short8 xf[4], yf[4];
-#pragma unroll
-        for (int mt = 0; mt < 4; ++mt)
-            xf[mt] = *(short8*)(&sX[xoff[h][mt]]);
-#pragma unroll
-        for (int nt = 0; nt < 4; ++nt)
-            yf[nt] = *(short8*)(&sY[yoff[h][nt]]);
-#pragma unroll
-        for (int mt = 0; mt < 4; ++mt)
-#pragma unroll
-            for (int nt = 0; nt < 4; ++nt)
-                acc[mt][nt] = __builtin_amdgcn_mfma_f32_16x16x32_bf16(
-                    xf[mt], yf[nt], acc[mt][nt], 0, 0, 0);
-    }
-
-    float sy[4];
-#pragma unroll
-    for (int nt = 0; nt < 4; ++nt)
-        sy[nt] = sqY[by + wn * 64 + nt * 16 + lrow];
-    float s = 0.f;
-#pragma unroll
-    for (int mt = 0; mt < 4; ++mt)
-#pragma unroll
-        for (int r = 0; r < 4; ++r) {
-            float sx = sqX[bx + wm * 64 + mt * 16 + lq * 4 + r];
-#pragma unroll
-            for (int nt = 0; nt < 4; ++nt)
-                s += __expf((2.0f * acc[mt][nt][r] - sx - sy[nt]) * (1.0f / 4096.0f));
-        }
-    s *= w;
-#pragma unroll
-    for (int off = 32; off; off >>= 1) s += __shfl_xor(s, off);
-    if ((tid & 63) == 0) red[tid >> 6] = s;
-    __syncthreads();
-    if (tid == 0) atomicAdd(accum + pair * 8, red[0] + red[1] + red[2] + red[3]);
-}
-
-__global__ __launch_bounds__(256) void k_ln64_red(
-        const float* __restrict__ part, int npart,
-        const float* __restrict__ bias, const float* __restrict__ g,
-        const float* __restrict__ b, float* __restrict__ outf,
-        ushort* __restrict__ outb, float* __restrict__ sq_l) {
-    int wave = threadIdx.x >> 6, lane = threadIdx.x & 63;
-    int row = blockIdx.x * 4 + wave;
-    float x = bias[lane];
-    for (int s = 0; s < npart; ++s)
-        x += part[(size_t)s * 4096 * 64 + row * 64 + lane];
-    float s = x;
-#pragma unroll
-    for (int off = 32; off; off >>= 1) s += __shfl_xor(s, off);
-    float mu = s * (1.0f / 64.0f);
-    float d = x - mu;
-    float v = d * d;
-#pragma unroll
-    for (int off = 32; off; off >>= 1) v += __shfl_xor(v, off);
-    float rs = rsqrtf(v * (1.0f / 64.0f) + 1e-9f);
-    float y = d * rs * g[lane] + b[lane];
-    outf[row * 64 + lane] = y;
-    outb[row * 64 + lane] = bf16r(y);
-    float q = y * y;
-#pragma unroll
-    for (int off = 32; off; off >>= 1) q += __shfl_xor(q, off);
-    if (lane == 0) sq_l[row] = q;
-}
-
-__global__ __launch_bounds__(256) void k_ln1024_red(
-        const float* __restrict__ p0, const float* __restrict__ p1,
-        const float* __restrict__ bias, const float* __restrict__ g,
-        const float* __restrict__ b, float* __restrict__ out) {
-    __shared__ float red[4];
-    int row = blockIdx.x, tid = threadIdx.x;
-    const float4 v0 = *(const float4*)(p0 + (size_t)row * 1024 + tid * 4);
-    const float4 v1 = *(const float4*)(p1 + (size_t)row * 1024 + tid * 4);
-    const float4 bb = *(const float4*)(bias + tid * 4);
-    float4 v;
-    v.x = v0.x + v1.x + bb.x;
-    v.y = v0.y + v1.y + bb.y;
-    v.z = v0.z + v1.z + bb.z;
-    v.w = v0.w + v1.w + bb.w;
-    float s = v.x + v.y + v.z + v.w;
-#pragma unroll
-    for (int off = 32; off; off >>= 1) s += __shfl_xor(s, off);
-    if ((tid & 63) == 0) red[tid >> 6] = s;
-    __syncthreads();
-    float mu = (red[0] + red[1] + red[2] + red[3]) * (1.0f / 1024.0f);
-    float dx = v.x - mu, dy = v.y - mu, dz = v.z - mu, dw = v.w - mu;
-    float q = dx * dx + dy * dy + dz * dz + dw * dw;
-#pragma unroll
-    for (int off = 32; off; off >>= 1) q += __shfl_xor(q, off);
-    __syncthreads();
-    if ((tid & 63) == 0) red[tid >> 6] = q;
-    __syncthreads();
-    float rs = rsqrtf((red[0] + red[1] + red[2] + red[3]) * (1.0f / 1024.0f) + 1e-9f);
-    const float4 gv = *(const float4*)(g + tid * 4);
-    const float4 bv = *(const float4*)(b + tid * 4);
-    float4 o;
-    o.x = dx * rs * gv.x + bv.x;
-    o.y = dy * rs * gv.y + bv.y;
-    o.z = dz * rs * gv.z + bv.z;
-    o.w = dw * rs * gv.w + bv.w;
-    *(float4*)(out + (size_t)row * 1024 + tid * 4) = o;
-}
-
-__global__ void k_finalize(const float* __restrict__ accum, float* __restrict__ out) {
-    out[0] = (accum[0] + accum[8] - 2.0f * accum[16]) * (64.0f / (4096.0f * 4096.0f));
 }
 
 extern "C" void kernel_launch(void* const* d_in, const int* in_sizes, int n_in,
@@ -747,8 +694,8 @@
     ushort* A1bf = (ushort*)(ws + 0);
     ushort* W1t  = (ushort*)(ws + 8 * MB);
     float*  h4p0 = (float*)(ws + 0);
+    float*  part = (float*)(ws + 16 * MB);
     ushort* H1bf = (ushort*)(ws + 16 * MB);
-    float*  part = (float*)(ws + 16 * MB);
     ushort* W4t  = (ushort*)(ws + 48 * MB);
     ushort* W2t  = (ushort*)(ws + 56 * MB);
     ushort* W3t  = (ushort*)(ws + 56 * MB + 512 * 1024);
@@ -758,22 +705,17 @@
     float*  acc3 = (float*)(ws + 59 * MB + 32768);
     ushort* Tbf  = (ushort*)(ws + 59 * MB + 65536);
 
-    k_pre<<<8704, 256, 0, stream>>>(hidden, A1bf, tsamp, Tbf, sq_t, acc3,
-                                    enc_w1, W1t, enc_w2, W2t,
-                                    dec_w1, W3t, dec_w2, W4t);
-
-    k_gemm1f<<<dim3(16, 16, 1), 512, 0, stream>>>(
-        A1bf, W1t, enc_b1, W2t, part, 4096, 4096, 1024);
-    k_ln64_red<<<1024, 256, 0, stream>>>(part, 16, enc_b2, enc_ln_g, enc_ln_b,
-                                         latent_f, Lbf, sq_l);
-
-    k_gemm<64, 0, false><<<dim3(64, 32, 1), 256, 0, stream>>>(
-        Lbf, W3t, dec_b1, H1bf, nullptr, 4096, 4096, 64, 64);
-    k_gemm256mb<128, 2, 8, 4><<<dim3(8, 16, 2), 512, 0, stream>>>(
-        H1bf, W4t, nullptr, h4p0, recon, 4096, 1024, 4096, 2048);
-    k_ln1024_red<<<4096, 256, 0, stream>>>(h4p0, recon, dec_b2, dec_ln_g,
-                                           dec_ln_b, recon);
-
-    k_gram_all<<<2080, 256, 0, stream>>>(Tbf, Lbf, sq_t, sq_l, acc3);
-    k_finalize<<<1, 1, 0, stream>>>(acc3, reg);
+    void* args[] = {
+        (void*)&hidden, (void*)&tsamp,
+        (void*)&enc_w1, (void*)&enc_b1, (void*)&enc_w2, (void*)&enc_b2,
+        (void*)&enc_ln_g, (void*)&enc_ln_b,
+        (void*)&dec_w1, (void*)&dec_b1, (void*)&dec_w2, (void*)&dec_b2,
+        (void*)&dec_ln_g, (void*)&dec_ln_b,
+        (void*)&recon, (void*)&latent_f, (void*)&reg,
+        (void*)&A1bf, (void*)&W1t, (void*)&part, (void*)&h4p0,
+        (void*)&H1bf, (void*)&W4t, (void*)&W2t, (void*)&W3t,
+        (void*)&Lbf, (void*)&sq_t, (void*)&sq_l, (void*)&acc3, (void*)&Tbf
+    };
+    hipLaunchCooperativeKernel((void*)k_mega, dim3(256), dim3(512),
+                               args, 0, stream);
 }
```

Measured after the change: 807.7 us. +210.0%, slower.
